# Kernel tuning notes

Hardware: AMD Instinct MI355X
Metric: run time of the kernel (lower is better)

## Reference

```python
import jax, jax.numpy as jnp
import numpy as np

J = 8      # number of octaves/scales
Q = 8      # first-order wavelets per octave (Q2 = 1 for second order)
T = 65536  # signal support
EPS = 1e-8
XI_MAX = 0.35  # highest wavelet center frequency (cycles/sample)


def _build_filters(N=T, J_=J, Q_=Q):
    """Morlet-like analytic filterbank defined directly in the Fourier domain."""
    f = np.fft.fftfreq(N)  # normalized freqs in [-0.5, 0.5)
    # first-order: J*Q log-spaced bandpass filters
    xis1 = XI_MAX * 2.0 ** (-np.arange(J_ * Q_) / Q_)
    sig1 = xis1 / Q_
    psi1 = np.exp(-0.5 * ((f[None, :] - xis1[:, None]) / sig1[:, None]) ** 2)
    j1 = np.arange(J_ * Q_) // Q_  # octave index of each first-order filter
    # second-order: one wavelet per octave (Q2=1)
    xis2 = XI_MAX * 2.0 ** (-np.arange(J_).astype(np.float64))
    sig2 = 0.6 * xis2
    psi2 = np.exp(-0.5 * ((f[None, :] - xis2[:, None]) / sig2[:, None]) ** 2)
    # low-pass at scale 2^J
    sig_phi = XI_MAX * 2.0 ** (-J_)
    phi = np.exp(-0.5 * (f / sig_phi) ** 2)
    return (jnp.asarray(psi1, jnp.float32), jnp.asarray(psi2, jnp.float32),
            jnp.asarray(phi, jnp.float32), j1)


def _scatter(x):
    """Order-0/1/2 wavelet scattering: FFT conv -> modulus -> low-pass -> subsample."""
    psi1, psi2, phi, j1 = _build_filters()
    stride = 2 ** J
    xf = jnp.fft.fft(x)  # [B, N] complex64
    lowpass = lambda uf: jnp.real(jnp.fft.ifft(uf * phi))[..., ::stride]
    S0 = lowpass(xf)[:, None, :]                                  # [B, 1, N/2^J]
    U1 = jnp.abs(jnp.fft.ifft(xf[:, None, :] * psi1[None]))      # [B, JQ, N]
    U1f = jnp.fft.fft(U1)
    S1 = lowpass(U1f)                                             # [B, JQ, N/2^J]
    parts = [S0, S1]
    for j2_ in range(J):  # small fixed loop over second-order scales
        sel = j1 < j2_    # static (numpy) frequency-ordering mask
        if not sel.any():
            continue
        U2 = jnp.abs(jnp.fft.ifft(U1f[:, sel] * psi2[j2_]))
        parts.append(lowpass(jnp.fft.fft(U2)))
    return jnp.concatenate(parts, axis=1)  # [B, 289, N/2^J]


def setup_inputs() -> dict:
    key = jax.random.key(0)
    x = jax.random.normal(key, (8, T), dtype=jnp.float32)
    return {"x": x}


def reference(x):
    Sx = _scatter(x)
    # kymatio Scattering1D has no `output_format` attr -> real=Sx, imag=0,
    # then log-magnitude normalization (normalize=True):
    mag = jnp.sqrt(Sx * Sx + EPS)
    real = jnp.log(mag + EPS)
    imag = jnp.zeros_like(real)
    return (real, imag)
```

## Files before the change

kernel.cpp:

```cpp
#include <hip/hip_runtime.h>
#include <hip/hip_fp16.h>
#include <math.h>

#define NN 65536
#define TWO_PI 6.283185307179586f
#define RSTR 264
#define SWZ(m) ((m) ^ (((m) >> 4) & 15))
#define SWZI(m, r) (SWZ(m) ^ ((r) & 12))
#define CTOT 10829824ul

__constant__ int CLO[8]  = {-32768, -15360, -5376, -8192, -8192, -2048, -2048, -2048};
__constant__ int CWW[8]  = {65536, 42240, 16384, 16384, 16384, 4096, 4096, 4096};
__constant__ int CRING[8] = {0, 0, 1, 1, 1, 1, 1, 1};
__constant__ unsigned long COFF[8] = {0ul, 4194304ul, 6897664ul, 7946240ul,
                                      8994816ul, 10043392ul, 10305536ul, 10567680ul};

__device__ __forceinline__ void lds_fence() {
    asm volatile("s_waitcnt lgkmcnt(0)" ::: "memory");
}
__device__ __forceinline__ int rev16(int p) { return ((p & 3) << 2) | (p >> 2); }
__device__ __forceinline__ int rev64(int p) { return ((p & 3) << 4) | (p & 12) | (p >> 4); }

__device__ __forceinline__ int quarter_mask(int klo, int khi)
{
    int qm = 0;
#pragma unroll
    for (int qq = 0; qq < 4; ++qq) {
        int lo_q = 16384 * qq - 255;
        int hi_q = 16384 * qq + 16639;
        bool act;
        if (klo >= 0) act = (hi_q >= klo) && (lo_q <= khi);
        else          act = (lo_q <= khi) || (hi_q >= klo + NN);
        if (act) qm |= (1 << qq);
    }
    return qm;
}

__device__ __forceinline__ void build_tw6(float* twt, int t)
{
    if (t < 16) {
        float s1, c1; __sincosf((TWO_PI / 64.0f) * (float)t, &s1, &c1);
        float c2 = c1 * c1 - s1 * s1, s2 = 2.f * c1 * s1;
        float c3 = c2 * c1 - s2 * s1, s3 = c2 * s1 + s2 * c1;
        float* e = twt + 6 * t;
        e[0] = c1; e[1] = s1; e[2] = c2; e[3] = s2; e[4] = c3; e[5] = s3;
    }
}

template<int SIGN>
__device__ __forceinline__ void fft16(float* xr, float* xi, float* yr, float* yi)
{
    const float S = (SIGN > 0) ? 1.0f : -1.0f;
    const float C8 = 0.92387953251f, S8 = 0.38268343236f, R2 = 0.70710678119f;
#pragma unroll
    for (int n0 = 0; n0 < 4; ++n0) {
        float z0r=xr[n0],    z0i=xi[n0];
        float z1r=xr[n0+4],  z1i=xi[n0+4];
        float z2r=xr[n0+8],  z2i=xi[n0+8];
        float z3r=xr[n0+12], z3i=xi[n0+12];
        float t0r=z0r+z2r, t0i=z0i+z2i;
        float t1r=z0r-z2r, t1i=z0i-z2i;
        float t2r=z1r+z3r, t2i=z1i+z3i;
        float t3r=S*(z1r-z3r), t3i=S*(z1i-z3i);
        xr[n0]=t0r+t2r;      xi[n0]=t0i+t2i;
        xr[n0+4]=t1r-t3i;    xi[n0+4]=t1i+t3r;
        xr[n0+8]=t0r-t2r;    xi[n0+8]=t0i-t2i;
        xr[n0+12]=t1r+t3i;   xi[n0+12]=t1i-t3r;
    }
    {
        const float W1r=C8,  W1i=S*S8;
        const float W2r=R2,  W2i=S*R2;
        const float W3r=S8,  W3i=S*C8;
        const float W6r=-R2, W6i=S*R2;
        const float W9r=-C8, W9i=-S*S8;
#define TWID(idx, wr, wi) { float ar=xr[idx], ai=xi[idx]; xr[idx]=ar*(wr)-ai*(wi); xi[idx]=ar*(wi)+ai*(wr); }
        TWID(5,W1r,W1i)  TWID(9,W2r,W2i)   TWID(13,W3r,W3i)
        TWID(6,W2r,W2i)  { float ar=xr[10], ai=xi[10]; xr[10]=-S*ai; xi[10]=S*ar; } TWID(14,W6r,W6i)
        TWID(7,W3r,W3i)  TWID(11,W6r,W6i)  TWID(15,W9r,W9i)
#undef TWID
    }
#pragma unroll
    for (int p = 0; p < 4; ++p) {
        float z0r=xr[4*p],   z0i=xi[4*p];
        float z1r=xr[4*p+1], z1i=xi[4*p+1];
        float z2r=xr[4*p+2], z2i=xi[4*p+2];
        float z3r=xr[4*p+3], z3i=xi[4*p+3];
        float t0r=z0r+z2r, t0i=z0i+z2i;
        float t1r=z0r-z2r, t1i=z0i-z2i;
        float t2r=z1r+z3r, t2i=z1i+z3i;
        float t3r=S*(z1r-z3r), t3i=S*(z1i-z3i);
        yr[p]=t0r+t2r;     yi[p]=t0i+t2i;
        yr[p+4]=t1r-t3i;   yi[p+4]=t1i+t3r;
        yr[p+8]=t0r-t2r;   yi[p+8]=t0i-t2i;
        yr[p+12]=t1r+t3i;  yi[p+12]=t1i-t3r;
    }
}

template<int SIGN, bool BIGTW, int OUT, bool INREAL, int PADL, int PADR>
__device__ __forceinline__ void fft256_soa(float* rr, float* ri, int u, int n1,
                                           float twrate, float mscale, int cxor, int qmask)
{
    float xr[16], xi[16], yr[16], yi[16];
#pragma unroll
    for (int qq = 0; qq < 4; ++qq) {
        if (qmask & (1 << qq)) {
#pragma unroll
            for (int j = 0; j < 4; ++j) {
                int b = qq * 4 + j;
                int s = SWZ(u + (b << 4)) ^ cxor;
                xr[b] = rr[s];
                xi[b] = INREAL ? 0.f : ri[s];
            }
        } else {
#pragma unroll
            for (int j = 0; j < 4; ++j) { xr[qq * 4 + j] = 0.f; xi[qq * 4 + j] = 0.f; }
        }
    }
    fft16<SIGN>(xr, xi, yr, yi);
    float sa, ca;
    __sincosf((float)SIGN * (TWO_PI / 256.0f) * (float)u, &sa, &ca);
    float twr = 1.f, twi = 0.f;
#pragma unroll
    for (int c = 0; c < 16; ++c) {
        int s = SWZ((c << 4) + u) ^ cxor;
        rr[s] = yr[c] * twr - yi[c] * twi;
        ri[s] = yr[c] * twi + yi[c] * twr;
        float nr = twr * ca - twi * sa; twi = twr * sa + twi * ca; twr = nr;
    }
    lds_fence();
#pragma unroll
    for (int a = 0; a < 16; ++a) {
        int s = SWZ((u << 4) + a) ^ cxor;
        xr[a] = rr[s]; xi[a] = ri[s];
    }
    fft16<SIGN>(xr, xi, yr, yi);
    float tbr = 1.f, tbi = 0.f, str = 1.f, sti = 0.f;
    if (BIGTW) {
        float s0, c0, s1, c1;
        __sincosf((float)SIGN * twrate * (float)(n1 * u), &s0, &c0);
        __sincosf((float)SIGN * twrate * (float)(n1 << 4), &s1, &c1);
        tbr = c0; tbi = s0; str = c1; sti = s1;
    }
#pragma unroll
    for (int d = 0; d < 16; ++d) {
        float vr = yr[d], vi = yi[d];
        if (BIGTW) {
            float pr = vr * tbr - vi * tbi, pi = vr * tbi + vi * tbr;
            vr = pr; vi = pi;
            float nr = tbr * str - tbi * sti; tbi = tbr * sti + tbi * str; tbr = nr;
        }
        int k = u + (d << 4);
        if (OUT == 1) {
            rr[SWZ(k) ^ cxor] = sqrtf(fmaf(vr, vr, vi * vi)) * mscale;
        } else if (OUT == 2) {
            float mag = sqrtf(fmaf(vr, vr, vi * vi)) * mscale;
            ri[PADL + k] = mag;
            if (k >= 256 - PADL) ri[k - (256 - PADL)] = mag;
            if (k < PADR) ri[PADL + 256 + k] = mag;
        } else {
            int s = SWZ(k) ^ cxor;
            rr[s] = vr; ri[s] = vi;
        }
    }
    lds_fence();
}

template<int L, int CLOG, int RST, int SIGN, bool SWZC>
__device__ __forceinline__ void lds_dit(float* re, float* im, const float* twt, int t, int T)
{
    const float S = (float)SIGN;
    const int NC = 1 << CLOG;
    const int nbf = NC * (L >> 2);
    for (int h = 1; h < L; h <<= 2) {
        __syncthreads();
        for (int i = t; i < nbf; i += T) {
            int c = i & (NC - 1);
            int bf = i >> CLOG;
            int j = bf & (h - 1);
            int q0 = ((bf - j) << 2) + j;
            int r0 = q0, r1 = q0 + h, r2 = q0 + 2 * h, r3 = q0 + 3 * h;
            int a0, a1, a2, a3;
            if (SWZC) {
                a0 = r0 * RST + SWZI(c, r0); a1 = r1 * RST + SWZI(c, r1);
                a2 = r2 * RST + SWZI(c, r2); a3 = r3 * RST + SWZI(c, r3);
            } else {
                a0 = r0 * RST + c; a1 = r1 * RST + c; a2 = r2 * RST + c; a3 = r3 * RST + c;
            }
            float x0r = re[a0], x0i = im[a0];
            float x1r = re[a1], x1i = im[a1];
            float x2r = re[a2], x2i = im[a2];
            float x3r = re[a3], x3i = im[a3];
            if (h > 1) {
                const float* e = twt + 6 * (j * (16 / h));
                float cj = e[0], sj = S * e[1];
                float c2 = e[2], s2 = S * e[3];
                float c3 = e[4], s3 = S * e[5];
                float r;
                r = x1r * cj - x1i * sj; x1i = x1r * sj + x1i * cj; x1r = r;
                r = x2r * c2 - x2i * s2; x2i = x2r * s2 + x2i * c2; x2r = r;
                r = x3r * c3 - x3i * s3; x3i = x3r * s3 + x3i * c3; x3r = r;
            }
            float t0r = x0r + x2r, t0i = x0i + x2i;
            float t1r = x0r - x2r, t1i = x0i - x2i;
            float t2r = x1r + x3r, t2i = x1i + x3i;
            float t3r = -S * (x1i - x3i), t3i = S * (x1r - x3r);
            re[a0] = t0r + t2r; im[a0] = t0i + t2i;
            re[a1] = t1r + t3r; im[a1] = t1i + t3i;
            re[a2] = t0r - t2r; im[a2] = t0i - t2i;
            re[a3] = t1r - t3r; im[a3] = t1i - t3i;
        }
    }
    __syncthreads();
}

template<int L, int CLOG, int RST, int SIGN, bool SWZC>
__device__ __forceinline__ void lds_dif(float* re, float* im, const float* twt, int t, int T)
{
    const float S = (float)SIGN;
    const int NC = 1 << CLOG;
    const int nbf = NC * (L >> 2);
    for (int h = L >> 2; h >= 1; h >>= 2) {
        __syncthreads();
        for (int i = t; i < nbf; i += T) {
            int c = i & (NC - 1);
            int bf = i >> CLOG;
            int j = bf & (h - 1);
            int q0 = ((bf - j) << 2) + j;
            int r0 = q0, r1 = q0 + h, r2 = q0 + 2 * h, r3 = q0 + 3 * h;
            int a0, a1, a2, a3;
            if (SWZC) {
                a0 = r0 * RST + SWZI(c, r0); a1 = r1 * RST + SWZI(c, r1);
                a2 = r2 * RST + SWZI(c, r2); a3 = r3 * RST + SWZI(c, r3);
            } else {
                a0 = r0 * RST + c; a1 = r1 * RST + c; a2 = r2 * RST + c; a3 = r3 * RST + c;
            }
            float x0r = re[a0], x0i = im[a0];
            float x1r = re[a1], x1i = im[a1];
            float x2r = re[a2], x2i = im[a2];
            float x3r = re[a3], x3i = im[a3];
            float t0r = x0r + x2r, t0i = x0i + x2i;
            float t1r = x0r - x2r, t1i = x0i - x2i;
            float t2r = x1r + x3r, t2i = x1i + x3i;
            float t3r = -S * (x1i - x3i), t3i = S * (x1r - x3r);
            float y1r = t1r + t3r, y1i = t1i + t3i;
            float y2r = t0r - t2r, y2i = t0i - t2i;
            float y3r = t1r - t3r, y3i = t1i - t3i;
            re[a0] = t0r + t2r; im[a0] = t0i + t2i;
            if (h > 1) {
                const float* e = twt + 6 * (j * (16 / h));
                float cj = e[0], sj = S * e[1];
                float c2 = e[2], s2 = S * e[3];
                float c3 = e[4], s3 = S * e[5];
                re[a1] = y1r * cj - y1i * sj; im[a1] = y1r * sj + y1i * cj;
                re[a2] = y2r * c2 - y2i * s2; im[a2] = y2r * s2 + y2i * c2;
                re[a3] = y3r * c3 - y3i * s3; im[a3] = y3r * s3 + y3i * c3;
            } else {
                re[a1] = y1r; im[a1] = y1i;
                re[a2] = y2r; im[a2] = y2i;
                re[a3] = y3r; im[a3] = y3i;
            }
        }
    }
    __syncthreads();
}

__global__ __launch_bounds__(256)
void xf_stage1(const float* __restrict__ x, float2* __restrict__ D)
{
    __shared__ float sre[16 * RSTR];
    __shared__ float sim[16 * RSTR];
    const int t = threadIdx.x;
    const int r = blockIdx.x >> 4;
    const int n10 = (blockIdx.x & 15) << 4;
#pragma unroll
    for (int it = 0; it < 16; ++it) {
        int flat = it * 256 + t;
        int i = flat & 15, n2 = flat >> 4;
        int n = (n10 + i) + (n2 << 8);
        sre[i * RSTR + SWZI(n2, i)] = x[(size_t)r * NN + n];
        sim[i * RSTR + SWZI(n2, i)] = 0.f;
    }
    __syncthreads();
    const int g = t >> 4, u = t & 15;
    fft256_soa<-1, true, 0, false, 0, 0>(sre + g * RSTR, sim + g * RSTR, u, n10 + g,
                                         TWO_PI / (float)NN, 1.f, g & 12, 15);
    __syncthreads();
#pragma unroll
    for (int it = 0; it < 16; ++it) {
        int flat = it * 256 + t;
        int i = flat & 15, k2 = flat >> 4;
        int s = i * RSTR + SWZI(k2, i);
        D[(size_t)r * NN + (k2 << 8) + (n10 + i)] = make_float2(sre[s], sim[s]);
    }
}

__global__ __launch_bounds__(256)
void xf_stage2(const float2* __restrict__ D, float2* __restrict__ XF)
{
    __shared__ float sre[16 * RSTR];
    __shared__ float sim[16 * RSTR];
    const int t = threadIdx.x;
    const int r = blockIdx.x >> 4;
    const int k20 = (blockIdx.x & 15) << 4;
#pragma unroll
    for (int it = 0; it < 16; ++it) {
        float2 v = D[(size_t)r * NN + ((size_t)(k20 + it) << 8) + t];
        sre[it * RSTR + SWZI(t, it)] = v.x;
        sim[it * RSTR + SWZI(t, it)] = v.y;
    }
    __syncthreads();
    const int g = t >> 4, u = t & 15;
    fft256_soa<-1, false, 0, false, 0, 0>(sre + g * RSTR, sim + g * RSTR, u, 0, 0.f, 1.f, g & 12, 15);
    __syncthreads();
#pragma unroll
    for (int it = 0; it < 16; ++it) {
        int flat = it * 256 + t;
        int fi = flat & 15, k1 = flat >> 4;
        int s = fi * RSTR + SWZI(k1, fi);
        XF[(size_t)r * NN + (size_t)(k20 + fi) + ((size_t)k1 << 8)] = make_float2(sre[s], sim[s]);
    }
}

__device__ void d_fo_stage1(float* sm, int t, int blk, const float2* __restrict__ XF,
                            __half2* __restrict__ Dh)
{
    float* sre = sm; float* sim = sm + 4224;
    const int r = blk >> 4;
    const int n10 = (blk & 15) << 4;
    const int q = r;
    const int j1 = q >> 6, ql = q & 63;
    const int srow = ql >> 3, w = ql & 7;
    const int lam = j1 * 8 + w;
    const float xi = 0.35f * exp2f(-(float)lam * 0.125f);
    const float invsig = 8.0f / xi;
    const float kc = xi * (float)NN;
    const float Hh = 5.0f * (xi * 0.125f) * (float)NN;
    const int klo = (int)(kc - Hh), khi = (int)(kc + Hh) + 1;
    const int qm = (khi >= NN) ? 15 : quarter_mask(klo, khi);
#pragma unroll
    for (int it = 0; it < 16; ++it) {
        int i = t & 15, n2 = (it << 4) + (t >> 4);
        if (!(qm & (1 << (it >> 2)))) {
            sre[i * RSTR + SWZI(n2, i)] = 0.f;
            sim[i * RSTR + SWZI(n2, i)] = 0.f;
            continue;
        }
        int n = (n10 + i) + (n2 << 8);
        float nsf = (float)((n < NN / 2) ? n : n - NN);
        float vr = 0.f, vi = 0.f;
        if (fabsf(nsf - kc) <= Hh) {
            float2 v = XF[(size_t)srow * NN + n];
            float a = (nsf * (1.0f / (float)NN) - xi) * invsig;
            float wg = __expf(-0.5f * a * a) * 0.0625f;
            vr = v.x * wg; vi = v.y * wg;
        }
        sre[i * RSTR + SWZI(n2, i)] = vr;
        sim[i * RSTR + SWZI(n2, i)] = vi;
    }
    __syncthreads();
    const int g = t >> 4, u = t & 15;
    fft256_soa<1, true, 0, false, 0, 0>(sre + g * RSTR, sim + g * RSTR, u, n10 + g,
                                        TWO_PI / (float)NN, 1.f, g & 12, qm);
    __syncthreads();
#pragma unroll
    for (int it = 0; it < 16; ++it) {
        int flat = it * 256 + t;
        int i = flat & 15, k2 = flat >> 4;
        int s = i * RSTR + SWZI(k2, i);
        Dh[(size_t)r * NN + (k2 << 8) + (n10 + i)] = __floats2half2_rn(sre[s], sim[s]);
    }
}

__device__ void d_fo_mid(float* sm, int t, int blk, const __half2* __restrict__ Dh,
                         __half2* __restrict__ D2h)
{
    float* sre = sm; float* sim = sm + 4224;
    const int r = blk >> 4;
    const int k20 = (blk & 15) << 4;
#pragma unroll
    for (int it = 0; it < 16; ++it) {
        float2 v = __half22float2(Dh[(size_t)r * NN + ((size_t)(k20 + it) << 8) + t]);
        sre[it * RSTR + SWZI(t, it)] = v.x;
        sim[it * RSTR + SWZI(t, it)] = v.y;
    }
    __syncthreads();
    const int g = t >> 4, u = t & 15;
    float* rr = sre + g * RSTR; float* ri = sim + g * RSTR;
    fft256_soa<1, false, 1, false, 0, 0>(rr, ri, u, 0, 0.f, 16.0f / (float)NN, g & 12, 15);
    fft256_soa<-1, true, 0, true, 0, 0>(rr, ri, u, k20 + g, TWO_PI / (float)NN, 1.f, g & 12, 15);
    __syncthreads();
#pragma unroll
    for (int it = 0; it < 16; ++it) {
        int flat = it * 256 + t;
        int i = flat & 15, k2 = flat >> 4;
        int s = i * RSTR + SWZI(k2, i);
        D2h[(size_t)r * NN + (k2 << 8) + (k20 + i)] = __floats2half2_rn(sre[s], sim[s]);
    }
}

__device__ void d_fo_stage2(float* sm, int t, int blk, const __half2* __restrict__ D2h,
                            __half2* __restrict__ Cw)
{
    float* sre = sm; float* sim = sm + 4224;
    const int r = blk >> 4;
    const int k20 = (blk & 15) << 4;
    const int j1 = r >> 6, ql = r & 63;
#pragma unroll
    for (int it = 0; it < 16; ++it) {
        float2 v = __half22float2(D2h[(size_t)r * NN + ((size_t)(k20 + it) << 8) + t]);
        sre[it * RSTR + SWZI(t, it)] = v.x;
        sim[it * RSTR + SWZI(t, it)] = v.y;
    }
    __syncthreads();
    const int g = t >> 4, u = t & 15;
    fft256_soa<-1, false, 0, false, 0, 0>(sre + g * RSTR, sim + g * RSTR, u, 0, 0.f, 1.f, g & 12, 15);
    __syncthreads();
    const size_t base = COFF[j1] + (size_t)ql * CWW[j1];
    const int lo = CLO[j1], Wd = CWW[j1];
#pragma unroll
    for (int it = 0; it < 16; ++it) {
        int flat = it * 256 + t;
        int fi = flat & 15, k1 = flat >> 4;
        int k = (k20 + fi) + (k1 << 8);
        int ksg = (k < NN / 2) ? k : k - NN;
        int idx = ksg - lo;
        if (idx >= 0 && idx < Wd) {
            int s = fi * RSTR + SWZI(k1, fi);
            Cw[base + idx] = __floats2half2_rn(sre[s], sim[s]);
        }
    }
}

__device__ void d_sfold(float* sm, int t, int blk, const float2* __restrict__ XF,
                        const __half2* __restrict__ Cw, float* __restrict__ out)
{
    float* Gr = sm; float* Gi = sm + 256;
    const float invsigphi = 731.428571f;
    float ar = 0.f, ai = 0.f;
    if (blk < 8) {
#pragma unroll
        for (int qq = -4; qq <= 4; ++qq) {
            int ks = t + (qq << 8);
            int k = ks & (NN - 1);
            float a = ((float)ks * (1.0f / (float)NN)) * invsigphi;
            float wg = __expf(-0.5f * a * a);
            float2 v = XF[(size_t)blk * NN + k];
            ar = fmaf(v.x, wg, ar); ai = fmaf(v.y, wg, ai);
        }
    } else {
        int q = blk - 8;
        int j1 = q >> 6, ql = q & 63;
        size_t base = COFF[j1] + (size_t)ql * CWW[j1];
        int lo = CLO[j1], Wd = CWW[j1], ring = CRING[j1];
#pragma unroll
        for (int qq = -4; qq <= 4; ++qq) {
            int ks = t + (qq << 8);
            float a = ((float)ks * (1.0f / (float)NN)) * invsigphi;
            float wg = __expf(-0.5f * a * a);
            int idx = ring ? ((ks - lo) & (Wd - 1)) : (ks - lo);
            float2 v = __half22float2(Cw[base + idx]);
            ar = fmaf(v.x, wg, ar); ai = fmaf(v.y, wg, ai);
        }
    }
    Gr[t] = ar; Gi[t] = ai;
    __syncthreads();
    float sb, cb;
    __sincosf((TWO_PI / 256.0f) * (float)t, &sb, &cb);
    float wr = 1.f, wi = 0.f, s = 0.f;
    for (int kk = 0; kk < 256; ++kk) {
        s = fmaf(Gr[kk], wr, s);
        s = fmaf(-Gi[kk], wi, s);
        float nr = wr * cb - wi * sb; wi = wr * sb + wi * cb; wr = nr;
    }
    s *= (1.0f / (float)NN);
    float mag = sqrtf(fmaf(s, s, 1e-8f));
    float val = logf(mag + 1e-8f);
    int b, chan;
    if (blk < 8) { b = blk; chan = 0; }
    else { int q = blk - 8; int j1 = q >> 6, ql = q & 63; b = ql >> 3; chan = 1 + j1 * 8 + (ql & 7); }
    out[((size_t)b * 289 + chan) * 256 + t] = val;
}

__device__ __forceinline__ void so_decode_full(int q, int& j1, int& j2, int& rb)
{
    int pp = q >> 6;
    rb = q & 63;
    j2 = (pp == 0) ? 1 : 2;
    j1 = (pp == 0) ? 0 : pp - 1;
}
__device__ __forceinline__ void so_decode_dec16(int q, int& j1, int& j2, int& rb)
{
    int pp = q >> 6;
    rb = q & 63;
    j2 = (pp < 3) ? 3 : 4;
    j1 = (pp < 3) ? pp : pp - 3;
}

__device__ void d_so_stage1(float* sm, int t, int blk, const __half2* __restrict__ Cw,
                            __half2* __restrict__ Dh)
{
    float* sre = sm; float* sim = sm + 4224;
    const int r = blk >> 4;
    const int n10 = (blk & 15) << 4;
    int j1, j2, rb;
    so_decode_full(r, j1, j2, rb);
    const float xi2 = 0.35f * exp2f(-(float)j2);
    const float invsig = 1.0f / (0.6f * xi2);
    const float kc = xi2 * (float)NN;
    const float Hh = 5.0f * (0.6f * xi2) * (float)NN;
    const int klo = (int)(kc - Hh), khi = (int)(kc + Hh) + 1;
    const int qm = (klo >= 0 && khi >= NN) ? 15 : quarter_mask(klo, khi);
    const size_t base = COFF[j1] + (size_t)rb * CWW[j1];
    const int lo = CLO[j1], Wd = CWW[j1];
#pragma unroll
    for (int it = 0; it < 16; ++it) {
        int i = t & 15, n2 = (it << 4) + (t >> 4);
        if (!(qm & (1 << (it >> 2)))) {
            sre[i * RSTR + SWZI(n2, i)] = 0.f;
            sim[i * RSTR + SWZI(n2, i)] = 0.f;
            continue;
        }
        int n = (n10 + i) + (n2 << 8);
        int ksg = (n < NN / 2) ? n : n - NN;
        float nsf = (float)ksg;
        float vr = 0.f, vi = 0.f;
        int idx = ksg - lo;
        if (fabsf(nsf - kc) <= Hh && idx >= 0 && idx < Wd) {
            float2 v = __half22float2(Cw[base + idx]);
            float a = (nsf * (1.0f / (float)NN) - xi2) * invsig;
            float wg = __expf(-0.5f * a * a) * (1.0f / 256.0f);
            vr = v.x * wg; vi = v.y * wg;
        }
        sre[i * RSTR + SWZI(n2, i)] = vr;
        sim[i * RSTR + SWZI(n2, i)] = vi;
    }
    __syncthreads();
    const int g = t >> 4, u = t & 15;
    fft256_soa<1, true, 0, false, 0, 0>(sre + g * RSTR, sim + g * RSTR, u, n10 + g,
                                        TWO_PI / (float)NN, 1.f, g & 12, qm);
    __syncthreads();
#pragma unroll
    for (int it = 0; it < 16; ++it) {
        int flat = it * 256 + t;
        int i = flat & 15, k2 = flat >> 4;
        int s = i * RSTR + SWZI(k2, i);
        Dh[(size_t)r * NN + (k2 << 8) + (n10 + i)] = __floats2half2_rn(sre[s], sim[s]);
    }
}

__device__ void d_so_stage2(float* sm, int t, int blk, const __half2* __restrict__ Dh,
                            float* __restrict__ S2acc)
{
    float* sre = sm; float* sim = sm + 4224;
    float* wtab = sm + 8448;
    const int r = blk >> 4;
    const int k20 = (blk & 15) << 4;
#pragma unroll
    for (int it = 0; it < 16; ++it) {
        float2 v = __half22float2(Dh[(size_t)r * NN + ((size_t)(k20 + it) << 8) + t]);
        sre[it * RSTR + SWZI(t, it)] = v.x;
        sim[it * RSTR + SWZI(t, it)] = v.y;
    }
    if (t < 128) {
        int fi = t >> 3, dd = (t & 7) - 4;
        int w = k20 + fi + (dd << 8) + 768;
        float val = 0.f;
        if (w >= 0 && w <= 1536) {
            float m = (float)(w - 768);
            val = 0.003426963f * __expf(-3.690276e-5f * m * m);
        }
        wtab[fi * 8 + (t & 7)] = val;
    }
    __syncthreads();
    const int g = t >> 4, u = t & 15;
    fft256_soa<1, false, 2, false, 4, 3>(sre + g * RSTR, sim + g * RSTR, u, 0, 0.f, 1.f, g & 12, 15);
    __syncthreads();
    float acc = 0.f;
#pragma unroll
    for (int fi = 0; fi < 16; ++fi) {
        const float* row = sim + fi * RSTR;
#pragma unroll
        for (int dd = 0; dd < 8; ++dd)
            acc = fmaf(row[t + dd], wtab[fi * 8 + dd], acc);
    }
    atomicAdd(&S2acc[(size_t)r * 256 + t], acc * (1.0f / 256.0f));
}

template<int MODE>
__device__ void d_dec16_s1(float* sm, int t, int blk, const float2* __restrict__ XF,
                           const __half2* __restrict__ Cw, __half2* __restrict__ Dh16)
{
    float* sre = sm; float* sim = sm + 4096; float* twt = sm + 8192;
    const int r = blk >> 2;
    const int c0 = (blk & 3) << 6;
    const int q = r;
    float xi, invsig, kc, Hh; int srow = 0; size_t cbase = 0; int lo = 0, Wd = 0, ring = 0;
    if (MODE == 1) {
        int j1 = 2 + (q >> 6); int ql = q & 63; srow = ql >> 3;
        int lam = j1 * 8 + (ql & 7);
        xi = 0.35f * exp2f(-(float)lam * 0.125f);
        invsig = 8.0f / xi; kc = xi * (float)NN; Hh = 6.10f * (xi * 0.125f) * (float)NN;
    } else {
        int j1, j2, rb;
        so_decode_dec16(q, j1, j2, rb);
        xi = 0.35f * exp2f(-(float)j2);
        invsig = 1.0f / (0.6f * xi); kc = xi * (float)NN;
        Hh = fminf(6.10f * (0.6f * xi) * (float)NN, 7967.0f);
        cbase = COFF[j1] + (size_t)rb * CWW[j1]; lo = CLO[j1]; Wd = CWW[j1]; ring = CRING[j1];
    }
    build_tw6(twt, t);
    const int klo = (int)ceilf(kc - Hh);
#pragma unroll
    for (int it = 0; it < 16; ++it) {
        int flat = it * 256 + t;
        int c = flat & 63, n2 = flat >> 6;
        int kap = (c0 + c) + (n2 << 8);
        int kk = klo + (int)(((unsigned)(kap - klo)) & 16383u);
        float vr = 0.f, vi = 0.f;
        if (fabsf((float)kk - kc) <= Hh) {
            float2 v;
            bool ok = true;
            if (MODE == 1) v = XF[(size_t)srow * NN + (kk & (NN - 1))];
            else {
                int idx;
                if (ring) idx = (kk - lo) & (Wd - 1);
                else { idx = kk - lo; ok = (idx >= 0 && idx < Wd); }
                v = ok ? __half22float2(Cw[cbase + idx]) : make_float2(0.f, 0.f);
            }
            float a = ((float)kk * (1.0f / (float)NN) - xi) * invsig;
            float wg = __expf(-0.5f * a * a) * 0.015625f;
            vr = v.x * wg; vi = v.y * wg;
        }
        int p = rev64(n2);
        sre[(p << 6) + c] = vr;
        sim[(p << 6) + c] = vi;
    }
    lds_dit<64, 6, 64, 1, false>(sre, sim, twt, t, 256);
    {
        const int c = t & 63, r0 = t >> 6;
        float sA, cA, sD, cD;
        __sincosf((TWO_PI / 16384.0f) * (float)(r0 * (c0 + c)), &sA, &cA);
        __sincosf((TWO_PI / 16384.0f) * (float)(4 * (c0 + c)), &sD, &cD);
#pragma unroll
        for (int it = 0; it < 16; ++it) {
            int row = (it << 2) + r0;
            int a = (row << 6) + c;
            float rr = sre[a] * cA - sim[a] * sA;
            sim[a] = sre[a] * sA + sim[a] * cA; sre[a] = rr;
            float nc = cA * cD - sA * sD; sA = cA * sD + sA * cD; cA = nc;
        }
    }
    __syncthreads();
#pragma unroll
    for (int it = 0; it < 16; ++it) {
        int flat = it * 256 + t;
        int c = flat & 63, row = flat >> 6;
        Dh16[(size_t)r * 16384 + (row << 8) + (c0 + c)] =
            __floats2half2_rn(sre[(row << 6) + c], sim[(row << 6) + c]);
    }
}

__device__ void d_dec16_s2so(float* sm, int t, int blk, const __half2* __restrict__ Dh16,
                             float* __restrict__ S2acc)
{
    float* sre = sm; float* sim = sm + 4224;
    float* wtab = sm + 8448;
    const int r = blk >> 2;
    const int k2base = (blk & 3) << 4;
#pragma unroll
    for (int it = 0; it < 16; ++it) {
        float2 v = __half22float2(Dh16[(size_t)r * 16384 + ((k2base + it) << 8) + t]);
        sre[it * RSTR + SWZI(t, it)] = v.x;
        sim[it * RSTR + SWZI(t, it)] = v.y;
    }
    if (t < 96) {
        int p = t / 6, dl = t % 6;
        float w = (float)(256 * (dl - 2) - 4 * (k2base + p));
        wtab[p * 6 + dl] = 0.003426963f * __expf(-3.690276e-5f * w * w);
    }
    __syncthreads();
    const int g = t >> 4, u = t & 15;
    fft256_soa<1, false, 2, false, 3, 2>(sre + g * RSTR, sim + g * RSTR, u, 0, 0.f,
                                         64.0f / (float)NN, g & 12, 15);
    __syncthreads();
    float acc = 0.f;
#pragma unroll
    for (int p = 0; p < 16; ++p) {
        const float* row = sim + p * RSTR;
#pragma unroll
        for (int dl = 0; dl < 6; ++dl)
            acc = fmaf(row[t + 5 - dl], wtab[p * 6 + dl], acc);
    }
    atomicAdd(&S2acc[(size_t)(192 + r) * 256 + t], acc * 4.0f);
}

__device__ void d_dec16_s2fo(float* sm, int t, int blk, const __half2* __restrict__ Dh16,
                             __half2* __restrict__ D2h16)
{
    float* sre = sm; float* sim = sm + 4224;
    const int r = blk >> 2;
    const int k2base = (blk & 3) << 4;
#pragma unroll
    for (int it = 0; it < 16; ++it) {
        float2 v = __half22float2(Dh16[(size_t)r * 16384 + ((k2base + it) << 8) + t]);
        sre[it * RSTR + SWZI(t, it)] = v.x;
        sim[it * RSTR + SWZI(t, it)] = v.y;
    }
    __syncthreads();
    const int g = t >> 4, u = t & 15;
    float* rr = sre + g * RSTR; float* ri = sim + g * RSTR;
    fft256_soa<1, false, 1, false, 0, 0>(rr, ri, u, 0, 0.f, 256.0f / (float)NN, g & 12, 15);
    fft256_soa<-1, true, 0, true, 0, 0>(rr, ri, u, k2base + g, TWO_PI / 16384.0f, 1.f, g & 12, 15);
    __syncthreads();
#pragma unroll
    for (int it = 0; it < 16; ++it) {
        int a = it * RSTR + SWZI(t, it);
        D2h16[(size_t)r * 16384 + ((k2base + it) << 8) + t] = __floats2half2_rn(sre[a], sim[a]);
    }
}

__device__ void d_dec16_s3fo(float* sm, int t, int blk, const __half2* __restrict__ D2h16,
                             __half2* __restrict__ Cw)
{
    float* sre = sm; float* sim = sm + 4096; float* twt = sm + 8192;
    const int r = blk >> 2;
    const int c0 = (blk & 3) << 6;
    const int j1 = 2 + (r >> 6), ql = r & 63;
    build_tw6(twt, t);
#pragma unroll
    for (int it = 0; it < 16; ++it) {
        int flat = it * 256 + t;
        int c = flat & 63, m2 = flat >> 6;
        float2 v = __half22float2(D2h16[(size_t)r * 16384 + (m2 << 8) + (c0 + c)]);
        sre[(m2 << 6) + c] = v.x;
        sim[(m2 << 6) + c] = v.y;
    }
    lds_dif<64, 6, 64, -1, false>(sre, sim, twt, t, 256);
    const int lo = CLO[j1];
    const size_t rbase = COFF[j1] + (size_t)ql * 16384;
#pragma unroll
    for (int it = 0; it < 16; ++it) {
        int flat = it * 256 + t;
        int c = flat & 63, p = flat >> 6;
        int kap = (c0 + c) + (rev64(p) << 8);
        int ks = (kap < 8192) ? kap : kap - 16384;
        int idx = (ks - lo) & 16383;
        int a = (p << 6) + c;
        Cw[rbase + idx] = __floats2half2_rn(sre[a], sim[a]);
    }
}

__device__ void d_m4k_fo(float* sm, int t, int blk, const float2* __restrict__ XF,
                         __half2* __restrict__ Cw)
{
    float* sre = sm; float* sim = sm + 4224; float* twt = sm + 8448;
    const int q = blk;
    const int j1 = 5 + (q >> 6), ql = q & 63;
    const int srow = ql >> 3;
    const int lam = j1 * 8 + (ql & 7);
    const float xi = 0.35f * exp2f(-(float)lam * 0.125f);
    const float invsig = 8.0f / xi;
    const float kc = xi * (float)NN;
    const float Hh = 6.10f * (xi * 0.125f) * (float)NN;
    const int klo = (int)ceilf(kc - Hh);
    build_tw6(twt, t);
#pragma unroll
    for (int it = 0; it < 16; ++it) {
        int kap = t + (it << 8);
        int kk = klo + (int)(((unsigned)(kap - klo)) & 4095u);
        float vr = 0.f, vi = 0.f;
        if (fabsf((float)kk - kc) <= Hh) {
            float2 v = XF[(size_t)srow * NN + (kk & (NN - 1))];
            float a = ((float)kk * (1.0f / (float)NN) - xi) * invsig;
            float wg = __expf(-0.5f * a * a);
            vr = v.x * wg; vi = v.y * wg;
        }
        int p = rev16(it);
        sre[p * RSTR + SWZI(t, p)] = vr;
        sim[p * RSTR + SWZI(t, p)] = vi;
    }
    lds_dit<16, 8, RSTR, 1, true>(sre, sim, twt, t, 256);
    {
        float sD, cD; __sincosf((TWO_PI / 4096.0f) * (float)t, &sD, &cD);
        float cA = 1.f, sA = 0.f;
#pragma unroll
        for (int it = 0; it < 16; ++it) {
            int a = it * RSTR + SWZI(t, it);
            float rr = sre[a] * cA - sim[a] * sA;
            sim[a] = sre[a] * sA + sim[a] * cA; sre[a] = rr;
            float nc = cA * cD - sA * sD; sA = cA * sD + sA * cD; cA = nc;
        }
    }
    __syncthreads();
    const int g = t >> 4, u = t & 15;
    float* rr = sre + g * RSTR; float* ri = sim + g * RSTR;
    fft256_soa<1, false, 1, false, 0, 0>(rr, ri, u, 0, 0.f, 16.0f / (float)NN, g & 12, 15);
    fft256_soa<-1, true, 0, true, 0, 0>(rr, ri, u, g, TWO_PI / 4096.0f, 1.f, g & 12, 15);
    lds_dif<16, 8, RSTR, -1, true>(sre, sim, twt, t, 256);
    const int lo = CLO[j1];
    const size_t rbase = COFF[j1] + (size_t)ql * 4096;
#pragma unroll
    for (int it = 0; it < 16; ++it) {
        int kap = t + (rev16(it) << 8);
        int ks = (kap < 2048) ? kap : kap - 4096;
        int idx = (ks - lo) & 4095;
        int a = it * RSTR + SWZI(t, it);
        Cw[rbase + idx] = __floats2half2_rn(sre[a], sim[a]);
    }
}

__device__ void d_m4k_so(float* sm, int t, int blk, const __half2* __restrict__ Cw,
                         float* __restrict__ out)
{
    float* sre = sm; float* sim = sm + 4224;
    float* twt = sm + 8448; float* wtab = sm + 8544;
    const int q = blk;
    const int pp = q >> 6, rb = q & 63;
    int j1, j2;
    if (pp < 5)       { j2 = 5; j1 = pp; }
    else if (pp < 11) { j2 = 6; j1 = pp - 5; }
    else              { j2 = 7; j1 = pp - 11; }
    const float xi2 = 0.35f * exp2f(-(float)j2);
    const float invsig = 1.0f / (0.6f * xi2);
    const float kc = xi2 * (float)NN;
    const float Hh = fminf(6.10f * (0.6f * xi2) * (float)NN, 1823.0f);
    const int klo = (int)ceilf(kc - Hh);
    const size_t cbase = COFF[j1] + (size_t)rb * CWW[j1];
    const int lo = CLO[j1], Wd = CWW[j1], ring = CRING[j1];
    build_tw6(twt, t);
#pragma unroll
    for (int it = 0; it < 16; ++it) {
        int kap = t + (it << 8);
        int kk = klo + (int)(((unsigned)(kap - klo)) & 4095u);
        float vr = 0.f, vi = 0.f;
        if (fabsf((float)kk - kc) <= Hh) {
            int idx; bool ok = true;
            if (ring) idx = (kk - lo) & (Wd - 1);
            else { idx = kk - lo; ok = (idx >= 0 && idx < Wd); }
            if (ok) {
                float2 v = __half22float2(Cw[cbase + idx]);
                float a = ((float)kk * (1.0f / (float)NN) - xi2) * invsig;
                float wg = __expf(-0.5f * a * a);
                vr = v.x * wg; vi = v.y * wg;
            }
        }
        int p = rev16(it);
        sre[p * RSTR + SWZI(t, p)] = vr;
        sim[p * RSTR + SWZI(t, p)] = vi;
    }
    if (t < 96) {
        int p = t / 6, dl = t % 6;
        float w = (float)(256 * (dl - 2) - 16 * p);
        wtab[p * 6 + dl] = 0.003426963f * __expf(-3.690276e-5f * w * w);
    }
    lds_dit<16, 8, RSTR, 1, true>(sre, sim, twt, t, 256);
    {
        float sD, cD; __sincosf((TWO_PI / 4096.0f) * (float)t, &sD, &cD);
        float cA = 1.f, sA = 0.f;
#pragma unroll
        for (int it = 0; it < 16; ++it) {
            int a = it * RSTR + SWZI(t, it);
            float rr = sre[a] * cA - sim[a] * sA;
            sim[a] = sre[a] * sA + sim[a] * cA; sre[a] = rr;
            float nc = cA * cD - sA * sD; sA = cA * sD + sA * cD; cA = nc;
        }
    }
    __syncthreads();
    const int g = t >> 4, u = t & 15;
    fft256_soa<1, false, 2, false, 3, 2>(sre + g * RSTR, sim + g * RSTR, u, 0, 0.f,
                                         1.0f / (float)NN, g & 12, 15);
    __syncthreads();
    float acc = 0.f;
#pragma unroll
    for (int p = 0; p < 16; ++p) {
        const float* row = sim + p * RSTR;
#pragma unroll
        for (int dl = 0; dl < 6; ++dl)
            acc = fmaf(row[t + 5 - dl], wtab[p * 6 + dl], acc);
    }
    acc *= 16.0f;
    const int b = rb >> 3;
    const int chan = 65 + 4 * j2 * (j2 - 1) + j1 * 8 + (rb & 7);
    float mag = sqrtf(fmaf(acc, acc, 1e-8f));
    out[((size_t)b * 289 + chan) * 256 + t] = logf(mag + 1e-8f);
}

__global__ __launch_bounds__(256)
void fo_s1_kernel(const float2* __restrict__ XF, __half2* __restrict__ Cw,
                  __half2* __restrict__ DhB, __half2* __restrict__ Dh16)
{
    __shared__ float sm[8704];
    const int t = threadIdx.x;
    const int b = blockIdx.x;
    if (b < 192) d_m4k_fo(sm, t, b, XF, Cw);
    else if (b < 960) d_dec16_s1<1>(sm, t, b - 192, XF, nullptr, Dh16);
    else d_fo_stage1(sm, t, b - 960, XF, DhB);
}

__global__ __launch_bounds__(256)
void fo_s2_kernel(const __half2* __restrict__ DhB, const __half2* __restrict__ Dh16,
                  __half2* __restrict__ D2h, __half2* __restrict__ D2h16)
{
    __shared__ float sm[8704];
    const int t = threadIdx.x;
    const int b = blockIdx.x;
    if (b < 768) d_dec16_s2fo(sm, t, b, Dh16, D2h16);
    else d_fo_mid(sm, t, b - 768, DhB, D2h);
}

__global__ __launch_bounds__(256)
void fo_s3_kernel(const __half2* __restrict__ D2h, const __half2* __restrict__ D2h16,
                  __half2* __restrict__ Cw)
{
    __shared__ float sm[8704];
    const int t = threadIdx.x;
    const int b = blockIdx.x;
    if (b < 768) d_dec16_s3fo(sm, t, b, D2h16, Cw);
    else d_fo_stage2(sm, t, b - 768, D2h, Cw);
}

__global__ __launch_bounds__(256)
void so_1_kernel(const float2* __restrict__ XF, const __half2* __restrict__ Cw,
                 __half2* __restrict__ DhS, __half2* __restrict__ Dh16so,
                 float* __restrict__ out)
{
    __shared__ float sm[8704];
    const int t = threadIdx.x;
    const int b = blockIdx.x;
    if (b < 1152) d_m4k_so(sm, t, b, Cw, out);
    else if (b < 2944) d_dec16_s1<2>(sm, t, b - 1152, nullptr, Cw, Dh16so);
    else if (b < 6016) d_so_stage1(sm, t, b - 2944, Cw, DhS);
    else d_sfold(sm, t, b - 6016, XF, Cw, out);
}

__global__ __launch_bounds__(256)
void so_2_kernel(const __half2* __restrict__ DhS, const __half2* __restrict__ Dh16so,
                 float* __restrict__ S2acc)
{
    __shared__ float sm[8704];
    const int t = threadIdx.x;
    const int b = blockIdx.x;
    if (b < 1792) d_dec16_s2so(sm, t, b, Dh16so, S2acc);
    else d_so_stage2(sm, t, b - 1792, DhS, S2acc);
}

__global__ __launch_bounds__(256)
void s2final(const float* __restrict__ S2acc, float* __restrict__ out)
{
    const int q = blockIdx.x, n = threadIdx.x;
    int j1, j2, rb;
    if (q < 192) so_decode_full(q, j1, j2, rb);
    else         so_decode_dec16(q - 192, j1, j2, rb);
    const int b = rb >> 3;
    const int chan = 65 + 4 * j2 * (j2 - 1) + j1 * 8 + (rb & 7);
    float s = S2acc[(size_t)q * 256 + n];
    float mag = sqrtf(fmaf(s, s, 1e-8f));
    out[((size_t)b * 289 + chan) * 256 + n] = logf(mag + 1e-8f);
}

__global__ void zero2_kernel(float* a, int na, float* b, int nb)
{
    int i = blockIdx.x * 256 + threadIdx.x;
    if (i < na) a[i] = 0.f;
    else if (i < na + nb) b[i - na] = 0.f;
}

extern "C" void kernel_launch(void* const* d_in, const int* in_sizes, int n_in,
                              void* d_out, int out_size, void* d_ws, size_t ws_size,
                              hipStream_t stream)
{
    const float* x = (const float*)d_in[0];
    float* out = (float*)d_out;
    char* ws = (char*)d_ws;

    size_t off = 0;
    float2*  XF    = (float2*)ws;                 off += 8ul * NN * 8;
    __half2* Cw    = (__half2*)(ws + off);        off += CTOT * 4ul;
    float*   S2acc = (float*)(ws + off);          off += 640ul * 256 * 4;
    off = (off + 255) & ~255ul;
    char* sc = ws + off;

    __half2* DhB   = (__half2*)sc;
    __half2* D2h   = (__half2*)(sc + 33554432ul);
    __half2* Dh16  = (__half2*)(sc + 67108864ul);
    __half2* D2h16 = (__half2*)(sc + 79691776ul);
    __half2* DhS    = (__half2*)sc;
    __half2* Dh16so = (__half2*)(sc + 50331648ul);
    float2*  Df     = (float2*)sc;

    {
        int nz = 8 * 289 * 256;
        int na = 640 * 256;
        zero2_kernel<<<(nz + na + 255) / 256, 256, 0, stream>>>(out + nz, nz, S2acc, na);
    }

    xf_stage1<<<8 * 16, 256, 0, stream>>>(x, Df);
    xf_stage2<<<8 * 16, 256, 0, stream>>>(Df, XF);

    fo_s1_kernel<<<3008, 256, 0, stream>>>(XF, Cw, DhB, Dh16);
    fo_s2_kernel<<<2816, 256, 0, stream>>>(DhB, Dh16, D2h, D2h16);
    fo_s3_kernel<<<2816, 256, 0, stream>>>(D2h, D2h16, Cw);

    so_1_kernel<<<6536, 256, 0, stream>>>(XF, Cw, DhS, Dh16so, out);
    so_2_kernel<<<4864, 256, 0, stream>>>(DhS, Dh16so, S2acc);
    s2final<<<640, 256, 0, stream>>>(S2acc, out);
}
```

Before: 257.6 us.

## Store FFT scratch in LDS as packed half2 and fold zeroing into first FFT

The intermediate FFT stages now keep their data in shared memory as packed __half2 values instead of split float real/imag arrays. This halves the LDS footprint, which goes from 8704 to 4480 floats per block, so more blocks can be resident per CU. It also lets global half2 data move to and from LDS with no conversion. Separately, the zeroing kernel is merged into the first input FFT kernel as extra blocks, which removes one launch. The cost is extra fp16 rounding at every intra-LDS butterfly pass, which lowers accuracy, plus convert instructions inside the FFT loops.

```diff
diff --git a/kernel.cpp b/kernel.cpp
--- a/kernel.cpp
+++ b/kernel.cpp
@@ -4,7 +4,7 @@
 
 #define NN 65536
 #define TWO_PI 6.283185307179586f
-#define RSTR 264
+#define HRSTR 264
 #define SWZ(m) ((m) ^ (((m) >> 4) & 15))
 #define SWZI(m, r) (SWZ(m) ^ ((r) & 12))
 #define CTOT 10829824ul
@@ -20,6 +20,10 @@
 }
 __device__ __forceinline__ int rev16(int p) { return ((p & 3) << 2) | (p >> 2); }
 __device__ __forceinline__ int rev64(int p) { return ((p & 3) << 4) | (p & 12) | (p >> 4); }
+__device__ __forceinline__ float2 h2f(__half2 h) { return __half22float2(h); }
+__device__ __forceinline__ __half2 f2h(float a, float b) {
+    return __floats2half2_rn(a, b);
+}
 
 __device__ __forceinline__ int quarter_mask(int klo, int khi)
 {
@@ -96,9 +100,9 @@
     }
 }
 
-template<int SIGN, bool BIGTW, int OUT, bool INREAL, int PADL, int PADR>
-__device__ __forceinline__ void fft256_soa(float* rr, float* ri, int u, int n1,
-                                           float twrate, float mscale, int cxor, int qmask)
+template<int SIGN, bool BIGTW, int OUT, int PADL, int PADR>
+__device__ __forceinline__ void fft256_pk(__half2* row, int u, int n1,
+                                          float twrate, float mscale, int cxor, int qmask)
 {
     float xr[16], xi[16], yr[16], yi[16];
 #pragma unroll
@@ -107,9 +111,8 @@
 #pragma unroll
             for (int j = 0; j < 4; ++j) {
                 int b = qq * 4 + j;
-                int s = SWZ(u + (b << 4)) ^ cxor;
-                xr[b] = rr[s];
-                xi[b] = INREAL ? 0.f : ri[s];
+                float2 v = h2f(row[SWZ(u + (b << 4)) ^ cxor]);
+                xr[b] = v.x; xi[b] = v.y;
             }
         } else {
 #pragma unroll
@@ -122,16 +125,15 @@
     float twr = 1.f, twi = 0.f;
 #pragma unroll
     for (int c = 0; c < 16; ++c) {
-        int s = SWZ((c << 4) + u) ^ cxor;
-        rr[s] = yr[c] * twr - yi[c] * twi;
-        ri[s] = yr[c] * twi + yi[c] * twr;
+        row[SWZ((c << 4) + u) ^ cxor] = f2h(yr[c] * twr - yi[c] * twi,
+                                            yr[c] * twi + yi[c] * twr);
         float nr = twr * ca - twi * sa; twi = twr * sa + twi * ca; twr = nr;
     }
     lds_fence();
 #pragma unroll
     for (int a = 0; a < 16; ++a) {
-        int s = SWZ((u << 4) + a) ^ cxor;
-        xr[a] = rr[s]; xi[a] = ri[s];
+        float2 v = h2f(row[SWZ((u << 4) + a) ^ cxor]);
+        xr[a] = v.x; xi[a] = v.y;
     }
     fft16<SIGN>(xr, xi, yr, yi);
     float tbr = 1.f, tbi = 0.f, str = 1.f, sti = 0.f;
@@ -151,22 +153,22 @@
         }
         int k = u + (d << 4);
         if (OUT == 1) {
-            rr[SWZ(k) ^ cxor] = sqrtf(fmaf(vr, vr, vi * vi)) * mscale;
+            row[SWZ(k) ^ cxor] = f2h(sqrtf(fmaf(vr, vr, vi * vi)) * mscale, 0.f);
         } else if (OUT == 2) {
             float mag = sqrtf(fmaf(vr, vr, vi * vi)) * mscale;
-            ri[PADL + k] = mag;
-            if (k >= 256 - PADL) ri[k - (256 - PADL)] = mag;
-            if (k < PADR) ri[PADL + 256 + k] = mag;
+            float* rf = (float*)row;
+            rf[PADL + k] = mag;
+            if (k >= 256 - PADL) rf[k - (256 - PADL)] = mag;
+            if (k < PADR) rf[PADL + 256 + k] = mag;
         } else {
-            int s = SWZ(k) ^ cxor;
-            rr[s] = vr; ri[s] = vi;
+            row[SWZ(k) ^ cxor] = f2h(vr, vi);
         }
     }
     lds_fence();
 }
 
 template<int L, int CLOG, int RST, int SIGN, bool SWZC>
-__device__ __forceinline__ void lds_dit(float* re, float* im, const float* twt, int t, int T)
+__device__ __forceinline__ void lds_dit_pk(__half2* pl, const float* twt, int t, int T)
 {
     const float S = (float)SIGN;
     const int NC = 1 << CLOG;
@@ -186,10 +188,10 @@
             } else {
                 a0 = r0 * RST + c; a1 = r1 * RST + c; a2 = r2 * RST + c; a3 = r3 * RST + c;
             }
-            float x0r = re[a0], x0i = im[a0];
-            float x1r = re[a1], x1i = im[a1];
-            float x2r = re[a2], x2i = im[a2];
-            float x3r = re[a3], x3i = im[a3];
+            float2 z0 = h2f(pl[a0]), z1 = h2f(pl[a1]);
+            float2 z2 = h2f(pl[a2]), z3 = h2f(pl[a3]);
+            float x0r=z0.x, x0i=z0.y, x1r=z1.x, x1i=z1.y;
+            float x2r=z2.x, x2i=z2.y, x3r=z3.x, x3i=z3.y;
             if (h > 1) {
                 const float* e = twt + 6 * (j * (16 / h));
                 float cj = e[0], sj = S * e[1];
@@ -204,17 +206,17 @@
             float t1r = x0r - x2r, t1i = x0i - x2i;
             float t2r = x1r + x3r, t2i = x1i + x3i;
             float t3r = -S * (x1i - x3i), t3i = S * (x1r - x3r);
-            re[a0] = t0r + t2r; im[a0] = t0i + t2i;
-            re[a1] = t1r + t3r; im[a1] = t1i + t3i;
-            re[a2] = t0r - t2r; im[a2] = t0i - t2i;
-            re[a3] = t1r - t3r; im[a3] = t1i - t3i;
+            pl[a0] = f2h(t0r + t2r, t0i + t2i);
+            pl[a1] = f2h(t1r + t3r, t1i + t3i);
+            pl[a2] = f2h(t0r - t2r, t0i - t2i);
+            pl[a3] = f2h(t1r - t3r, t1i - t3i);
         }
     }
     __syncthreads();
 }
 
 template<int L, int CLOG, int RST, int SIGN, bool SWZC>
-__device__ __forceinline__ void lds_dif(float* re, float* im, const float* twt, int t, int T)
+__device__ __forceinline__ void lds_dif_pk(__half2* pl, const float* twt, int t, int T)
 {
     const float S = (float)SIGN;
     const int NC = 1 << CLOG;
@@ -234,10 +236,10 @@
             } else {
                 a0 = r0 * RST + c; a1 = r1 * RST + c; a2 = r2 * RST + c; a3 = r3 * RST + c;
             }
-            float x0r = re[a0], x0i = im[a0];
-            float x1r = re[a1], x1i = im[a1];
-            float x2r = re[a2], x2i = im[a2];
-            float x3r = re[a3], x3i = im[a3];
+            float2 z0 = h2f(pl[a0]), z1 = h2f(pl[a1]);
+            float2 z2 = h2f(pl[a2]), z3 = h2f(pl[a3]);
+            float x0r=z0.x, x0i=z0.y, x1r=z1.x, x1i=z1.y;
+            float x2r=z2.x, x2i=z2.y, x3r=z3.x, x3i=z3.y;
             float t0r = x0r + x2r, t0i = x0i + x2i;
             float t1r = x0r - x2r, t1i = x0i - x2i;
             float t2r = x1r + x3r, t2i = x1i + x3i;
@@ -245,51 +247,108 @@
             float y1r = t1r + t3r, y1i = t1i + t3i;
             float y2r = t0r - t2r, y2i = t0i - t2i;
             float y3r = t1r - t3r, y3i = t1i - t3i;
-            re[a0] = t0r + t2r; im[a0] = t0i + t2i;
+            pl[a0] = f2h(t0r + t2r, t0i + t2i);
             if (h > 1) {
                 const float* e = twt + 6 * (j * (16 / h));
                 float cj = e[0], sj = S * e[1];
                 float c2 = e[2], s2 = S * e[3];
                 float c3 = e[4], s3 = S * e[5];
-                re[a1] = y1r * cj - y1i * sj; im[a1] = y1r * sj + y1i * cj;
-                re[a2] = y2r * c2 - y2i * s2; im[a2] = y2r * s2 + y2i * c2;
-                re[a3] = y3r * c3 - y3i * s3; im[a3] = y3r * s3 + y3i * c3;
+                pl[a1] = f2h(y1r * cj - y1i * sj, y1r * sj + y1i * cj);
+                pl[a2] = f2h(y2r * c2 - y2i * s2, y2r * s2 + y2i * c2);
+                pl[a3] = f2h(y3r * c3 - y3i * s3, y3r * s3 + y3i * c3);
             } else {
-                re[a1] = y1r; im[a1] = y1i;
-                re[a2] = y2r; im[a2] = y2i;
-                re[a3] = y3r; im[a3] = y3i;
+                pl[a1] = f2h(y1r, y1i);
+                pl[a2] = f2h(y2r, y2i);
+                pl[a3] = f2h(y3r, y3i);
             }
         }
     }
     __syncthreads();
 }
 
+template<int SIGN, bool BIGTW>
+__device__ __forceinline__ void fft256_f32(float* rr, float* ri, int u, int n1,
+                                           float twrate, int cxor)
+{
+    float xr[16], xi[16], yr[16], yi[16];
+#pragma unroll
+    for (int b = 0; b < 16; ++b) {
+        int s = SWZ(u + (b << 4)) ^ cxor;
+        xr[b] = rr[s]; xi[b] = ri[s];
+    }
+    fft16<SIGN>(xr, xi, yr, yi);
+    float sa, ca;
+    __sincosf((float)SIGN * (TWO_PI / 256.0f) * (float)u, &sa, &ca);
+    float twr = 1.f, twi = 0.f;
+#pragma unroll
+    for (int c = 0; c < 16; ++c) {
+        int s = SWZ((c << 4) + u) ^ cxor;
+        rr[s] = yr[c] * twr - yi[c] * twi;
+        ri[s] = yr[c] * twi + yi[c] * twr;
+        float nr = twr * ca - twi * sa; twi = twr * sa + twi * ca; twr = nr;
+    }
+    lds_fence();
+#pragma unroll
+    for (int a = 0; a < 16; ++a) {
+        int s = SWZ((u << 4) + a) ^ cxor;
+        xr[a] = rr[s]; xi[a] = ri[s];
+    }
+    fft16<SIGN>(xr, xi, yr, yi);
+    float tbr = 1.f, tbi = 0.f, str = 1.f, sti = 0.f;
+    if (BIGTW) {
+        float s0, c0, s1, c1;
+        __sincosf((float)SIGN * twrate * (float)(n1 * u), &s0, &c0);
+        __sincosf((float)SIGN * twrate * (float)(n1 << 4), &s1, &c1);
+        tbr = c0; tbi = s0; str = c1; sti = s1;
+    }
+#pragma unroll
+    for (int d = 0; d < 16; ++d) {
+        float vr = yr[d], vi = yi[d];
+        if (BIGTW) {
+            float pr = vr * tbr - vi * tbi, pi = vr * tbi + vi * tbr;
+            vr = pr; vi = pi;
+            float nr = tbr * str - tbi * sti; tbi = tbr * sti + tbi * str; tbr = nr;
+        }
+        int s = SWZ(u + (d << 4)) ^ cxor;
+        rr[s] = vr; ri[s] = vi;
+    }
+    lds_fence();
+}
+
 __global__ __launch_bounds__(256)
-void xf_stage1(const float* __restrict__ x, float2* __restrict__ D)
-{
-    __shared__ float sre[16 * RSTR];
-    __shared__ float sim[16 * RSTR];
+void xfz_kernel(const float* __restrict__ x, float2* __restrict__ D,
+                float* __restrict__ outImag, int nz, float* __restrict__ S2acc, int na)
+{
+    __shared__ float sre[16 * HRSTR];
+    __shared__ float sim[16 * HRSTR];
     const int t = threadIdx.x;
-    const int r = blockIdx.x >> 4;
-    const int n10 = (blockIdx.x & 15) << 4;
+    const int blk = blockIdx.x;
+    if (blk >= 128) {
+        int i = (blk - 128) * 256 + t;
+        if (i < nz) outImag[i] = 0.f;
+        else if (i < nz + na) S2acc[i - nz] = 0.f;
+        return;
+    }
+    const int r = blk >> 4;
+    const int n10 = (blk & 15) << 4;
 #pragma unroll
     for (int it = 0; it < 16; ++it) {
         int flat = it * 256 + t;
         int i = flat & 15, n2 = flat >> 4;
         int n = (n10 + i) + (n2 << 8);
-        sre[i * RSTR + SWZI(n2, i)] = x[(size_t)r * NN + n];
-        sim[i * RSTR + SWZI(n2, i)] = 0.f;
+        sre[i * HRSTR + SWZI(n2, i)] = x[(size_t)r * NN + n];
+        sim[i * HRSTR + SWZI(n2, i)] = 0.f;
     }
     __syncthreads();
     const int g = t >> 4, u = t & 15;
-    fft256_soa<-1, true, 0, false, 0, 0>(sre + g * RSTR, sim + g * RSTR, u, n10 + g,
-                                         TWO_PI / (float)NN, 1.f, g & 12, 15);
+    fft256_f32<-1, true>(sre + g * HRSTR, sim + g * HRSTR, u, n10 + g,
+                         TWO_PI / (float)NN, g & 12);
     __syncthreads();
 #pragma unroll
     for (int it = 0; it < 16; ++it) {
         int flat = it * 256 + t;
         int i = flat & 15, k2 = flat >> 4;
-        int s = i * RSTR + SWZI(k2, i);
+        int s = i * HRSTR + SWZI(k2, i);
         D[(size_t)r * NN + (k2 << 8) + (n10 + i)] = make_float2(sre[s], sim[s]);
     }
 }
@@ -297,38 +356,39 @@
 __global__ __launch_bounds__(256)
 void xf_stage2(const float2* __restrict__ D, float2* __restrict__ XF)
 {
-    __shared__ float sre[16 * RSTR];
-    __shared__ float sim[16 * RSTR];
+    __shared__ float sre[16 * HRSTR];
+    __shared__ float sim[16 * HRSTR];
     const int t = threadIdx.x;
     const int r = blockIdx.x >> 4;
     const int k20 = (blockIdx.x & 15) << 4;
 #pragma unroll
     for (int it = 0; it < 16; ++it) {
         float2 v = D[(size_t)r * NN + ((size_t)(k20 + it) << 8) + t];
-        sre[it * RSTR + SWZI(t, it)] = v.x;
-        sim[it * RSTR + SWZI(t, it)] = v.y;
+        sre[it * HRSTR + SWZI(t, it)] = v.x;
+        sim[it * HRSTR + SWZI(t, it)] = v.y;
     }
     __syncthreads();
     const int g = t >> 4, u = t & 15;
-    fft256_soa<-1, false, 0, false, 0, 0>(sre + g * RSTR, sim + g * RSTR, u, 0, 0.f, 1.f, g & 12, 15);
+    fft256_f32<-1, false>(sre + g * HRSTR, sim + g * HRSTR, u, 0, 0.f, g & 12);
     __syncthreads();
 #pragma unroll
     for (int it = 0; it < 16; ++it) {
         int flat = it * 256 + t;
         int fi = flat & 15, k1 = flat >> 4;
-        int s = fi * RSTR + SWZI(k1, fi);
+        int s = fi * HRSTR + SWZI(k1, fi);
         XF[(size_t)r * NN + (size_t)(k20 + fi) + ((size_t)k1 << 8)] = make_float2(sre[s], sim[s]);
     }
 }
 
-__device__ void d_fo_stage1(float* sm, int t, int blk, const float2* __restrict__ XF,
+#define SM_FLOATS 4480
+
+__device__ void d_fo_stage1(float* smf, int t, int blk, const float2* __restrict__ XF,
                             __half2* __restrict__ Dh)
 {
-    float* sre = sm; float* sim = sm + 4224;
+    __half2* sld = (__half2*)smf;
     const int r = blk >> 4;
     const int n10 = (blk & 15) << 4;
-    const int q = r;
-    const int j1 = q >> 6, ql = q & 63;
+    const int j1 = r >> 6, ql = r & 63;
     const int srow = ql >> 3, w = ql & 7;
     const int lam = j1 * 8 + w;
     const float xi = 0.35f * exp2f(-(float)lam * 0.125f);
@@ -341,8 +401,7 @@
     for (int it = 0; it < 16; ++it) {
         int i = t & 15, n2 = (it << 4) + (t >> 4);
         if (!(qm & (1 << (it >> 2)))) {
-            sre[i * RSTR + SWZI(n2, i)] = 0.f;
-            sim[i * RSTR + SWZI(n2, i)] = 0.f;
+            sld[i * HRSTR + SWZI(n2, i)] = f2h(0.f, 0.f);
             continue;
         }
         int n = (n10 + i) + (n2 << 8);
@@ -354,66 +413,57 @@
             float wg = __expf(-0.5f * a * a) * 0.0625f;
             vr = v.x * wg; vi = v.y * wg;
         }
-        sre[i * RSTR + SWZI(n2, i)] = vr;
-        sim[i * RSTR + SWZI(n2, i)] = vi;
+        sld[i * HRSTR + SWZI(n2, i)] = f2h(vr, vi);
     }
     __syncthreads();
     const int g = t >> 4, u = t & 15;
-    fft256_soa<1, true, 0, false, 0, 0>(sre + g * RSTR, sim + g * RSTR, u, n10 + g,
-                                        TWO_PI / (float)NN, 1.f, g & 12, qm);
+    fft256_pk<1, true, 0, 0, 0>(sld + g * HRSTR, u, n10 + g, TWO_PI / (float)NN, 1.f,
+                                g & 12, qm);
     __syncthreads();
 #pragma unroll
     for (int it = 0; it < 16; ++it) {
         int flat = it * 256 + t;
         int i = flat & 15, k2 = flat >> 4;
-        int s = i * RSTR + SWZI(k2, i);
-        Dh[(size_t)r * NN + (k2 << 8) + (n10 + i)] = __floats2half2_rn(sre[s], sim[s]);
-    }
-}
-
-__device__ void d_fo_mid(float* sm, int t, int blk, const __half2* __restrict__ Dh,
+        Dh[(size_t)r * NN + (k2 << 8) + (n10 + i)] = sld[i * HRSTR + SWZI(k2, i)];
+    }
+}
+
+__device__ void d_fo_mid(float* smf, int t, int blk, const __half2* __restrict__ Dh,
                          __half2* __restrict__ D2h)
 {
-    float* sre = sm; float* sim = sm + 4224;
+    __half2* sld = (__half2*)smf;
     const int r = blk >> 4;
     const int k20 = (blk & 15) << 4;
 #pragma unroll
-    for (int it = 0; it < 16; ++it) {
-        float2 v = __half22float2(Dh[(size_t)r * NN + ((size_t)(k20 + it) << 8) + t]);
-        sre[it * RSTR + SWZI(t, it)] = v.x;
-        sim[it * RSTR + SWZI(t, it)] = v.y;
-    }
+    for (int it = 0; it < 16; ++it)
+        sld[it * HRSTR + SWZI(t, it)] = Dh[(size_t)r * NN + ((size_t)(k20 + it) << 8) + t];
     __syncthreads();
     const int g = t >> 4, u = t & 15;
-    float* rr = sre + g * RSTR; float* ri = sim + g * RSTR;
-    fft256_soa<1, false, 1, false, 0, 0>(rr, ri, u, 0, 0.f, 16.0f / (float)NN, g & 12, 15);
-    fft256_soa<-1, true, 0, true, 0, 0>(rr, ri, u, k20 + g, TWO_PI / (float)NN, 1.f, g & 12, 15);
+    __half2* row = sld + g * HRSTR;
+    fft256_pk<1, false, 1, 0, 0>(row, u, 0, 0.f, 16.0f / (float)NN, g & 12, 15);
+    fft256_pk<-1, true, 0, 0, 0>(row, u, k20 + g, TWO_PI / (float)NN, 1.f, g & 12, 15);
     __syncthreads();
 #pragma unroll
     for (int it = 0; it < 16; ++it) {
         int flat = it * 256 + t;
         int i = flat & 15, k2 = flat >> 4;
-        int s = i * RSTR + SWZI(k2, i);
-        D2h[(size_t)r * NN + (k2 << 8) + (k20 + i)] = __floats2half2_rn(sre[s], sim[s]);
-    }
-}
-
-__device__ void d_fo_stage2(float* sm, int t, int blk, const __half2* __restrict__ D2h,
+        D2h[(size_t)r * NN + (k2 << 8) + (k20 + i)] = sld[i * HRSTR + SWZI(k2, i)];
+    }
+}
+
+__device__ void d_fo_stage2(float* smf, int t, int blk, const __half2* __restrict__ D2h,
                             __half2* __restrict__ Cw)
 {
-    float* sre = sm; float* sim = sm + 4224;
+    __half2* sld = (__half2*)smf;
     const int r = blk >> 4;
     const int k20 = (blk & 15) << 4;
     const int j1 = r >> 6, ql = r & 63;
 #pragma unroll
-    for (int it = 0; it < 16; ++it) {
-        float2 v = __half22float2(D2h[(size_t)r * NN + ((size_t)(k20 + it) << 8) + t]);
-        sre[it * RSTR + SWZI(t, it)] = v.x;
-        sim[it * RSTR + SWZI(t, it)] = v.y;
-    }
+    for (int it = 0; it < 16; ++it)
+        sld[it * HRSTR + SWZI(t, it)] = D2h[(size_t)r * NN + ((size_t)(k20 + it) << 8) + t];
     __syncthreads();
     const int g = t >> 4, u = t & 15;
-    fft256_soa<-1, false, 0, false, 0, 0>(sre + g * RSTR, sim + g * RSTR, u, 0, 0.f, 1.f, g & 12, 15);
+    fft256_pk<-1, false, 0, 0, 0>(sld + g * HRSTR, u, 0, 0.f, 1.f, g & 12, 15);
     __syncthreads();
     const size_t base = COFF[j1] + (size_t)ql * CWW[j1];
     const int lo = CLO[j1], Wd = CWW[j1];
@@ -424,17 +474,15 @@
         int k = (k20 + fi) + (k1 << 8);
         int ksg = (k < NN / 2) ? k : k - NN;
         int idx = ksg - lo;
-        if (idx >= 0 && idx < Wd) {
-            int s = fi * RSTR + SWZI(k1, fi);
-            Cw[base + idx] = __floats2half2_rn(sre[s], sim[s]);
-        }
-    }
-}
-
-__device__ void d_sfold(float* sm, int t, int blk, const float2* __restrict__ XF,
+        if (idx >= 0 && idx < Wd)
+            Cw[base + idx] = sld[fi * HRSTR + SWZI(k1, fi)];
+    }
+}
+
+__device__ void d_sfold(float* smf, int t, int blk, const float2* __restrict__ XF,
                         const __half2* __restrict__ Cw, float* __restrict__ out)
 {
-    float* Gr = sm; float* Gi = sm + 256;
+    float* Gr = smf; float* Gi = smf + 256;
     const float invsigphi = 731.428571f;
     float ar = 0.f, ai = 0.f;
     if (blk < 8) {
@@ -458,7 +506,7 @@
             float a = ((float)ks * (1.0f / (float)NN)) * invsigphi;
             float wg = __expf(-0.5f * a * a);
             int idx = ring ? ((ks - lo) & (Wd - 1)) : (ks - lo);
-            float2 v = __half22float2(Cw[base + idx]);
+            float2 v = h2f(Cw[base + idx]);
             ar = fmaf(v.x, wg, ar); ai = fmaf(v.y, wg, ai);
         }
     }
@@ -496,10 +544,10 @@
     j1 = (pp < 3) ? pp : pp - 3;
 }
 
-__device__ void d_so_stage1(float* sm, int t, int blk, const __half2* __restrict__ Cw,
+__device__ void d_so_stage1(float* smf, int t, int blk, const __half2* __restrict__ Cw,
                             __half2* __restrict__ Dh)
 {
-    float* sre = sm; float* sim = sm + 4224;
+    __half2* sld = (__half2*)smf;
     const int r = blk >> 4;
     const int n10 = (blk & 15) << 4;
     int j1, j2, rb;
@@ -516,8 +564,7 @@
     for (int it = 0; it < 16; ++it) {
         int i = t & 15, n2 = (it << 4) + (t >> 4);
         if (!(qm & (1 << (it >> 2)))) {
-            sre[i * RSTR + SWZI(n2, i)] = 0.f;
-            sim[i * RSTR + SWZI(n2, i)] = 0.f;
+            sld[i * HRSTR + SWZI(n2, i)] = f2h(0.f, 0.f);
             continue;
         }
         int n = (n10 + i) + (n2 << 8);
@@ -526,41 +573,36 @@
         float vr = 0.f, vi = 0.f;
         int idx = ksg - lo;
         if (fabsf(nsf - kc) <= Hh && idx >= 0 && idx < Wd) {
-            float2 v = __half22float2(Cw[base + idx]);
+            float2 v = h2f(Cw[base + idx]);
             float a = (nsf * (1.0f / (float)NN) - xi2) * invsig;
             float wg = __expf(-0.5f * a * a) * (1.0f / 256.0f);
             vr = v.x * wg; vi = v.y * wg;
         }
-        sre[i * RSTR + SWZI(n2, i)] = vr;
-        sim[i * RSTR + SWZI(n2, i)] = vi;
+        sld[i * HRSTR + SWZI(n2, i)] = f2h(vr, vi);
     }
     __syncthreads();
     const int g = t >> 4, u = t & 15;
-    fft256_soa<1, true, 0, false, 0, 0>(sre + g * RSTR, sim + g * RSTR, u, n10 + g,
-                                        TWO_PI / (float)NN, 1.f, g & 12, qm);
+    fft256_pk<1, true, 0, 0, 0>(sld + g * HRSTR, u, n10 + g, TWO_PI / (float)NN, 1.f,
+                                g & 12, qm);
     __syncthreads();
 #pragma unroll
     for (int it = 0; it < 16; ++it) {
         int flat = it * 256 + t;
         int i = flat & 15, k2 = flat >> 4;
-        int s = i * RSTR + SWZI(k2, i);
-        Dh[(size_t)r * NN + (k2 << 8) + (n10 + i)] = __floats2half2_rn(sre[s], sim[s]);
-    }
-}
-
-__device__ void d_so_stage2(float* sm, int t, int blk, const __half2* __restrict__ Dh,
+        Dh[(size_t)r * NN + (k2 << 8) + (n10 + i)] = sld[i * HRSTR + SWZI(k2, i)];
+    }
+}
+
+__device__ void d_so_stage2(float* smf, int t, int blk, const __half2* __restrict__ Dh,
                             float* __restrict__ S2acc)
 {
-    float* sre = sm; float* sim = sm + 4224;
-    float* wtab = sm + 8448;
+    __half2* sld = (__half2*)smf;
+    float* wtab = smf + 4320;
     const int r = blk >> 4;
     const int k20 = (blk & 15) << 4;
 #pragma unroll
-    for (int it = 0; it < 16; ++it) {
-        float2 v = __half22float2(Dh[(size_t)r * NN + ((size_t)(k20 + it) << 8) + t]);
-        sre[it * RSTR + SWZI(t, it)] = v.x;
-        sim[it * RSTR + SWZI(t, it)] = v.y;
-    }
+    for (int it = 0; it < 16; ++it)
+        sld[it * HRSTR + SWZI(t, it)] = Dh[(size_t)r * NN + ((size_t)(k20 + it) << 8) + t];
     if (t < 128) {
         int fi = t >> 3, dd = (t & 7) - 4;
         int w = k20 + fi + (dd << 8) + 768;
@@ -573,12 +615,12 @@
     }
     __syncthreads();
     const int g = t >> 4, u = t & 15;
-    fft256_soa<1, false, 2, false, 4, 3>(sre + g * RSTR, sim + g * RSTR, u, 0, 0.f, 1.f, g & 12, 15);
+    fft256_pk<1, false, 2, 4, 3>(sld + g * HRSTR, u, 0, 0.f, 1.f, g & 12, 15);
     __syncthreads();
     float acc = 0.f;
 #pragma unroll
     for (int fi = 0; fi < 16; ++fi) {
-        const float* row = sim + fi * RSTR;
+        const float* row = (const float*)(sld + fi * HRSTR);
 #pragma unroll
         for (int dd = 0; dd < 8; ++dd)
             acc = fmaf(row[t + dd], wtab[fi * 8 + dd], acc);
@@ -587,22 +629,22 @@
 }
 
 template<int MODE>
-__device__ void d_dec16_s1(float* sm, int t, int blk, const float2* __restrict__ XF,
+__device__ void d_dec16_s1(float* smf, int t, int blk, const float2* __restrict__ XF,
                            const __half2* __restrict__ Cw, __half2* __restrict__ Dh16)
 {
-    float* sre = sm; float* sim = sm + 4096; float* twt = sm + 8192;
+    __half2* sld = (__half2*)smf;
+    float* twt = smf + 4224;
     const int r = blk >> 2;
     const int c0 = (blk & 3) << 6;
-    const int q = r;
     float xi, invsig, kc, Hh; int srow = 0; size_t cbase = 0; int lo = 0, Wd = 0, ring = 0;
     if (MODE == 1) {
-        int j1 = 2 + (q >> 6); int ql = q & 63; srow = ql >> 3;
+        int j1 = 2 + (r >> 6); int ql = r & 63; srow = ql >> 3;
         int lam = j1 * 8 + (ql & 7);
         xi = 0.35f * exp2f(-(float)lam * 0.125f);
         invsig = 8.0f / xi; kc = xi * (float)NN; Hh = 6.10f * (xi * 0.125f) * (float)NN;
     } else {
         int j1, j2, rb;
-        so_decode_dec16(q, j1, j2, rb);
+        so_decode_dec16(r, j1, j2, rb);
         xi = 0.35f * exp2f(-(float)j2);
         invsig = 1.0f / (0.6f * xi); kc = xi * (float)NN;
         Hh = fminf(6.10f * (0.6f * xi) * (float)NN, 7967.0f);
@@ -625,17 +667,16 @@
                 int idx;
                 if (ring) idx = (kk - lo) & (Wd - 1);
                 else { idx = kk - lo; ok = (idx >= 0 && idx < Wd); }
-                v = ok ? __half22float2(Cw[cbase + idx]) : make_float2(0.f, 0.f);
+                v = ok ? h2f(Cw[cbase + idx]) : make_float2(0.f, 0.f);
             }
             float a = ((float)kk * (1.0f / (float)NN) - xi) * invsig;
             float wg = __expf(-0.5f * a * a) * 0.015625f;
             vr = v.x * wg; vi = v.y * wg;
         }
         int p = rev64(n2);
-        sre[(p << 6) + c] = vr;
-        sim[(p << 6) + c] = vi;
-    }
-    lds_dit<64, 6, 64, 1, false>(sre, sim, twt, t, 256);
+        sld[(p << 6) + c] = f2h(vr, vi);
+    }
+    lds_dit_pk<64, 6, 64, 1, false>(sld, twt, t, 256);
     {
         const int c = t & 63, r0 = t >> 6;
         float sA, cA, sD, cD;
@@ -645,8 +686,8 @@
         for (int it = 0; it < 16; ++it) {
             int row = (it << 2) + r0;
             int a = (row << 6) + c;
-            float rr = sre[a] * cA - sim[a] * sA;
-            sim[a] = sre[a] * sA + sim[a] * cA; sre[a] = rr;
+            float2 z = h2f(sld[a]);
+            sld[a] = f2h(z.x * cA - z.y * sA, z.x * sA + z.y * cA);
             float nc = cA * cD - sA * sD; sA = cA * sD + sA * cD; cA = nc;
         }
     }
@@ -655,24 +696,20 @@
     for (int it = 0; it < 16; ++it) {
         int flat = it * 256 + t;
         int c = flat & 63, row = flat >> 6;
-        Dh16[(size_t)r * 16384 + (row << 8) + (c0 + c)] =
-            __floats2half2_rn(sre[(row << 6) + c], sim[(row << 6) + c]);
-    }
-}
-
-__device__ void d_dec16_s2so(float* sm, int t, int blk, const __half2* __restrict__ Dh16,
+        Dh16[(size_t)r * 16384 + (row << 8) + (c0 + c)] = sld[(row << 6) + c];
+    }
+}
+
+__device__ void d_dec16_s2so(float* smf, int t, int blk, const __half2* __restrict__ Dh16,
                              float* __restrict__ S2acc)
 {
-    float* sre = sm; float* sim = sm + 4224;
-    float* wtab = sm + 8448;
+    __half2* sld = (__half2*)smf;
+    float* wtab = smf + 4320;
     const int r = blk >> 2;
     const int k2base = (blk & 3) << 4;
 #pragma unroll
-    for (int it = 0; it < 16; ++it) {
-        float2 v = __half22float2(Dh16[(size_t)r * 16384 + ((k2base + it) << 8) + t]);
-        sre[it * RSTR + SWZI(t, it)] = v.x;
-        sim[it * RSTR + SWZI(t, it)] = v.y;
-    }
+    for (int it = 0; it < 16; ++it)
+        sld[it * HRSTR + SWZI(t, it)] = Dh16[(size_t)r * 16384 + ((k2base + it) << 8) + t];
     if (t < 96) {
         int p = t / 6, dl = t % 6;
         float w = (float)(256 * (dl - 2) - 4 * (k2base + p));
@@ -680,13 +717,12 @@
     }
     __syncthreads();
     const int g = t >> 4, u = t & 15;
-    fft256_soa<1, false, 2, false, 3, 2>(sre + g * RSTR, sim + g * RSTR, u, 0, 0.f,
-                                         64.0f / (float)NN, g & 12, 15);
+    fft256_pk<1, false, 2, 3, 2>(sld + g * HRSTR, u, 0, 0.f, 64.0f / (float)NN, g & 12, 15);
     __syncthreads();
     float acc = 0.f;
 #pragma unroll
     for (int p = 0; p < 16; ++p) {
-        const float* row = sim + p * RSTR;
+        const float* row = (const float*)(sld + p * HRSTR);
 #pragma unroll
         for (int dl = 0; dl < 6; ++dl)
             acc = fmaf(row[t + 5 - dl], wtab[p * 6 + dl], acc);
@@ -694,35 +730,31 @@
     atomicAdd(&S2acc[(size_t)(192 + r) * 256 + t], acc * 4.0f);
 }
 
-__device__ void d_dec16_s2fo(float* sm, int t, int blk, const __half2* __restrict__ Dh16,
+__device__ void d_dec16_s2fo(float* smf, int t, int blk, const __half2* __restrict__ Dh16,
                              __half2* __restrict__ D2h16)
 {
-    float* sre = sm; float* sim = sm + 4224;
+    __half2* sld = (__half2*)smf;
     const int r = blk >> 2;
     const int k2base = (blk & 3) << 4;
 #pragma unroll
-    for (int it = 0; it < 16; ++it) {
-        float2 v = __half22float2(Dh16[(size_t)r * 16384 + ((k2base + it) << 8) + t]);
-        sre[it * RSTR + SWZI(t, it)] = v.x;
-        sim[it * RSTR + SWZI(t, it)] = v.y;
-    }
+    for (int it = 0; it < 16; ++it)
+        sld[it * HRSTR + SWZI(t, it)] = Dh16[(size_t)r * 16384 + ((k2base + it) << 8) + t];
     __syncthreads();
     const int g = t >> 4, u = t & 15;
-    float* rr = sre + g * RSTR; float* ri = sim + g * RSTR;
-    fft256_soa<1, false, 1, false, 0, 0>(rr, ri, u, 0, 0.f, 256.0f / (float)NN, g & 12, 15);
-    fft256_soa<-1, true, 0, true, 0, 0>(rr, ri, u, k2base + g, TWO_PI / 16384.0f, 1.f, g & 12, 15);
-    __syncthreads();
-#pragma unroll
-    for (int it = 0; it < 16; ++it) {
-        int a = it * RSTR + SWZI(t, it);
-        D2h16[(size_t)r * 16384 + ((k2base + it) << 8) + t] = __floats2half2_rn(sre[a], sim[a]);
-    }
-}
-
-__device__ void d_dec16_s3fo(float* sm, int t, int blk, const __half2* __restrict__ D2h16,
+    __half2* row = sld + g * HRSTR;
+    fft256_pk<1, false, 1, 0, 0>(row, u, 0, 0.f, 256.0f / (float)NN, g & 12, 15);
+    fft256_pk<-1, true, 0, 0, 0>(row, u, k2base + g, TWO_PI / 16384.0f, 1.f, g & 12, 15);
+    __syncthreads();
+#pragma unroll
+    for (int it = 0; it < 16; ++it)
+        D2h16[(size_t)r * 16384 + ((k2base + it) << 8) + t] = sld[it * HRSTR + SWZI(t, it)];
+}
+
+__device__ void d_dec16_s3fo(float* smf, int t, int blk, const __half2* __restrict__ D2h16,
                              __half2* __restrict__ Cw)
 {
-    float* sre = sm; float* sim = sm + 4096; float* twt = sm + 8192;
+    __half2* sld = (__half2*)smf;
+    float* twt = smf + 4224;
     const int r = blk >> 2;
     const int c0 = (blk & 3) << 6;
     const int j1 = 2 + (r >> 6), ql = r & 63;
@@ -731,11 +763,9 @@
     for (int it = 0; it < 16; ++it) {
         int flat = it * 256 + t;
         int c = flat & 63, m2 = flat >> 6;
-        float2 v = __half22float2(D2h16[(size_t)r * 16384 + (m2 << 8) + (c0 + c)]);
-        sre[(m2 << 6) + c] = v.x;
-        sim[(m2 << 6) + c] = v.y;
-    }
-    lds_dif<64, 6, 64, -1, false>(sre, sim, twt, t, 256);
+        sld[(m2 << 6) + c] = D2h16[(size_t)r * 16384 + (m2 << 8) + (c0 + c)];
+    }
+    lds_dif_pk<64, 6, 64, -1, false>(sld, twt, t, 256);
     const int lo = CLO[j1];
     const size_t rbase = COFF[j1] + (size_t)ql * 16384;
 #pragma unroll
@@ -745,17 +775,16 @@
         int kap = (c0 + c) + (rev64(p) << 8);
         int ks = (kap < 8192) ? kap : kap - 16384;
         int idx = (ks - lo) & 16383;
-        int a = (p << 6) + c;
-        Cw[rbase + idx] = __floats2half2_rn(sre[a], sim[a]);
-    }
-}
-
-__device__ void d_m4k_fo(float* sm, int t, int blk, const float2* __restrict__ XF,
+        Cw[rbase + idx] = sld[(p << 6) + c];
+    }
+}
+
+__device__ void d_m4k_fo(float* smf, int t, int blk, const float2* __restrict__ XF,
                          __half2* __restrict__ Cw)
 {
-    float* sre = sm; float* sim = sm + 4224; float* twt = sm + 8448;
-    const int q = blk;
-    const int j1 = 5 + (q >> 6), ql = q & 63;
+    __half2* sld = (__half2*)smf;
+    float* twt = smf + 4224;
+    const int j1 = 5 + (blk >> 6), ql = blk & 63;
     const int srow = ql >> 3;
     const int lam = j1 * 8 + (ql & 7);
     const float xi = 0.35f * exp2f(-(float)lam * 0.125f);
@@ -776,27 +805,26 @@
             vr = v.x * wg; vi = v.y * wg;
         }
         int p = rev16(it);
-        sre[p * RSTR + SWZI(t, p)] = vr;
-        sim[p * RSTR + SWZI(t, p)] = vi;
-    }
-    lds_dit<16, 8, RSTR, 1, true>(sre, sim, twt, t, 256);
+        sld[p * HRSTR + SWZI(t, p)] = f2h(vr, vi);
+    }
+    lds_dit_pk<16, 8, HRSTR, 1, true>(sld, twt, t, 256);
     {
         float sD, cD; __sincosf((TWO_PI / 4096.0f) * (float)t, &sD, &cD);
         float cA = 1.f, sA = 0.f;
 #pragma unroll
         for (int it = 0; it < 16; ++it) {
-            int a = it * RSTR + SWZI(t, it);
-            float rr = sre[a] * cA - sim[a] * sA;
-            sim[a] = sre[a] * sA + sim[a] * cA; sre[a] = rr;
+            int a = it * HRSTR + SWZI(t, it);
+            float2 z = h2f(sld[a]);
+            sld[a] = f2h(z.x * cA - z.y * sA, z.x * sA + z.y * cA);
             float nc = cA * cD - sA * sD; sA = cA * sD + sA * cD; cA = nc;
         }
     }
     __syncthreads();
     const int g = t >> 4, u = t & 15;
-    float* rr = sre + g * RSTR; float* ri = sim + g * RSTR;
-    fft256_soa<1, false, 1, false, 0, 0>(rr, ri, u, 0, 0.f, 16.0f / (float)NN, g & 12, 15);
-    fft256_soa<-1, true, 0, true, 0, 0>(rr, ri, u, g, TWO_PI / 4096.0f, 1.f, g & 12, 15);
-    lds_dif<16, 8, RSTR, -1, true>(sre, sim, twt, t, 256);
+    __half2* row = sld + g * HRSTR;
+    fft256_pk<1, false, 1, 0, 0>(row, u, 0, 0.f, 16.0f / (float)NN, g & 12, 15);
+    fft256_pk<-1, true, 0, 0, 0>(row, u, g, TWO_PI / 4096.0f, 1.f, g & 12, 15);
+    lds_dif_pk<16, 8, HRSTR, -1, true>(sld, twt, t, 256);
     const int lo = CLO[j1];
     const size_t rbase = COFF[j1] + (size_t)ql * 4096;
 #pragma unroll
@@ -804,18 +832,17 @@
         int kap = t + (rev16(it) << 8);
         int ks = (kap < 2048) ? kap : kap - 4096;
         int idx = (ks - lo) & 4095;
-        int a = it * RSTR + SWZI(t, it);
-        Cw[rbase + idx] = __floats2half2_rn(sre[a], sim[a]);
-    }
-}
-
-__device__ void d_m4k_so(float* sm, int t, int blk, const __half2* __restrict__ Cw,
+        Cw[rbase + idx] = sld[it * HRSTR + SWZI(t, it)];
+    }
+}
+
+__device__ void d_m4k_so(float* smf, int t, int blk, const __half2* __restrict__ Cw,
                          float* __restrict__ out)
 {
-    float* sre = sm; float* sim = sm + 4224;
-    float* twt = sm + 8448; float* wtab = sm + 8544;
-    const int q = blk;
-    const int pp = q >> 6, rb = q & 63;
+    __half2* sld = (__half2*)smf;
+    float* twt = smf + 4224;
+    float* wtab = smf + 4320;
+    const int pp = blk >> 6, rb = blk & 63;
     int j1, j2;
     if (pp < 5)       { j2 = 5; j1 = pp; }
     else if (pp < 11) { j2 = 6; j1 = pp - 5; }
@@ -838,42 +865,40 @@
             if (ring) idx = (kk - lo) & (Wd - 1);
             else { idx = kk - lo; ok = (idx >= 0 && idx < Wd); }
             if (ok) {
-                float2 v = __half22float2(Cw[cbase + idx]);
+                float2 v = h2f(Cw[cbase + idx]);
                 float a = ((float)kk * (1.0f / (float)NN) - xi2) * invsig;
                 float wg = __expf(-0.5f * a * a);
                 vr = v.x * wg; vi = v.y * wg;
             }
         }
         int p = rev16(it);
-        sre[p * RSTR + SWZI(t, p)] = vr;
-        sim[p * RSTR + SWZI(t, p)] = vi;
+        sld[p * HRSTR + SWZI(t, p)] = f2h(vr, vi);
     }
     if (t < 96) {
         int p = t / 6, dl = t % 6;
         float w = (float)(256 * (dl - 2) - 16 * p);
         wtab[p * 6 + dl] = 0.003426963f * __expf(-3.690276e-5f * w * w);
     }
-    lds_dit<16, 8, RSTR, 1, true>(sre, sim, twt, t, 256);
+    lds_dit_pk<16, 8, HRSTR, 1, true>(sld, twt, t, 256);
     {
         float sD, cD; __sincosf((TWO_PI / 4096.0f) * (float)t, &sD, &cD);
         float cA = 1.f, sA = 0.f;
 #pragma unroll
         for (int it = 0; it < 16; ++it) {
-            int a = it * RSTR + SWZI(t, it);
-            float rr = sre[a] * cA - sim[a] * sA;
-            sim[a] = sre[a] * sA + sim[a] * cA; sre[a] = rr;
+            int a = it * HRSTR + SWZI(t, it);
+            float2 z = h2f(sld[a]);
+            sld[a] = f2h(z.x * cA - z.y * sA, z.x * sA + z.y * cA);
             float nc = cA * cD - sA * sD; sA = cA * sD + sA * cD; cA = nc;
         }
     }
     __syncthreads();
     const int g = t >> 4, u = t & 15;
-    fft256_soa<1, false, 2, false, 3, 2>(sre + g * RSTR, sim + g * RSTR, u, 0, 0.f,
-                                         1.0f / (float)NN, g & 12, 15);
+    fft256_pk<1, false, 2, 3, 2>(sld + g * HRSTR, u, 0, 0.f, 1.0f / (float)NN, g & 12, 15);
     __syncthreads();
     float acc = 0.f;
 #pragma unroll
     for (int p = 0; p < 16; ++p) {
-        const float* row = sim + p * RSTR;
+        const float* row = (const float*)(sld + p * HRSTR);
 #pragma unroll
         for (int dl = 0; dl < 6; ++dl)
             acc = fmaf(row[t + 5 - dl], wtab[p * 6 + dl], acc);
@@ -889,34 +914,34 @@
 void fo_s1_kernel(const float2* __restrict__ XF, __half2* __restrict__ Cw,
                   __half2* __restrict__ DhB, __half2* __restrict__ Dh16)
 {
-    __shared__ float sm[8704];
+    __shared__ float smf[SM_FLOATS];
     const int t = threadIdx.x;
     const int b = blockIdx.x;
-    if (b < 192) d_m4k_fo(sm, t, b, XF, Cw);
-    else if (b < 960) d_dec16_s1<1>(sm, t, b - 192, XF, nullptr, Dh16);
-    else d_fo_stage1(sm, t, b - 960, XF, DhB);
+    if (b < 192) d_m4k_fo(smf, t, b, XF, Cw);
+    else if (b < 960) d_dec16_s1<1>(smf, t, b - 192, XF, nullptr, Dh16);
+    else d_fo_stage1(smf, t, b - 960, XF, DhB);
 }
 
 __global__ __launch_bounds__(256)
 void fo_s2_kernel(const __half2* __restrict__ DhB, const __half2* __restrict__ Dh16,
                   __half2* __restrict__ D2h, __half2* __restrict__ D2h16)
 {
-    __shared__ float sm[8704];
+    __shared__ float smf[SM_FLOATS];
     const int t = threadIdx.x;
     const int b = blockIdx.x;
-    if (b < 768) d_dec16_s2fo(sm, t, b, Dh16, D2h16);
-    else d_fo_mid(sm, t, b - 768, DhB, D2h);
+    if (b < 768) d_dec16_s2fo(smf, t, b, Dh16, D2h16);
+    else d_fo_mid(smf, t, b - 768, DhB, D2h);
 }
 
 __global__ __launch_bounds__(256)
 void fo_s3_kernel(const __half2* __restrict__ D2h, const __half2* __restrict__ D2h16,
                   __half2* __restrict__ Cw)
 {
-    __shared__ float sm[8704];
+    __shared__ float smf[SM_FLOATS];
     const int t = threadIdx.x;
     const int b = blockIdx.x;
-    if (b < 768) d_dec16_s3fo(sm, t, b, D2h16, Cw);
-    else d_fo_stage2(sm, t, b - 768, D2h, Cw);
+    if (b < 768) d_dec16_s3fo(smf, t, b, D2h16, Cw);
+    else d_fo_stage2(smf, t, b - 768, D2h, Cw);
 }
 
 __global__ __launch_bounds__(256)
@@ -924,24 +949,24 @@
                  __half2* __restrict__ DhS, __half2* __restrict__ Dh16so,
                  float* __restrict__ out)
 {
-    __shared__ float sm[8704];
+    __shared__ float smf[SM_FLOATS];
     const int t = threadIdx.x;
     const int b = blockIdx.x;
-    if (b < 1152) d_m4k_so(sm, t, b, Cw, out);
-    else if (b < 2944) d_dec16_s1<2>(sm, t, b - 1152, nullptr, Cw, Dh16so);
-    else if (b < 6016) d_so_stage1(sm, t, b - 2944, Cw, DhS);
-    else d_sfold(sm, t, b - 6016, XF, Cw, out);
+    if (b < 1152) d_m4k_so(smf, t, b, Cw, out);
+    else if (b < 2944) d_dec16_s1<2>(smf, t, b - 1152, nullptr, Cw, Dh16so);
+    else if (b < 6016) d_so_stage1(smf, t, b - 2944, Cw, DhS);
+    else d_sfold(smf, t, b - 6016, XF, Cw, out);
 }
 
 __global__ __launch_bounds__(256)
 void so_2_kernel(const __half2* __restrict__ DhS, const __half2* __restrict__ Dh16so,
                  float* __restrict__ S2acc)
 {
-    __shared__ float sm[8704];
+    __shared__ float smf[SM_FLOATS];
     const int t = threadIdx.x;
     const int b = blockIdx.x;
-    if (b < 1792) d_dec16_s2so(sm, t, b, Dh16so, S2acc);
-    else d_so_stage2(sm, t, b - 1792, DhS, S2acc);
+    if (b < 1792) d_dec16_s2so(smf, t, b, Dh16so, S2acc);
+    else d_so_stage2(smf, t, b - 1792, DhS, S2acc);
 }
 
 __global__ __launch_bounds__(256)
@@ -958,13 +983,6 @@
     out[((size_t)b * 289 + chan) * 256 + n] = logf(mag + 1e-8f);
 }
 
-__global__ void zero2_kernel(float* a, int na, float* b, int nb)
-{
-    int i = blockIdx.x * 256 + threadIdx.x;
-    if (i < na) a[i] = 0.f;
-    else if (i < na + nb) b[i - na] = 0.f;
-}
-
 extern "C" void kernel_launch(void* const* d_in, const int* in_sizes, int n_in,
                               void* d_out, int out_size, void* d_ws, size_t ws_size,
                               hipStream_t stream)
@@ -988,13 +1006,11 @@
     __half2* Dh16so = (__half2*)(sc + 50331648ul);
     float2*  Df     = (float2*)sc;
 
-    {
-        int nz = 8 * 289 * 256;
-        int na = 640 * 256;
-        zero2_kernel<<<(nz + na + 255) / 256, 256, 0, stream>>>(out + nz, nz, S2acc, na);
-    }
-
-    xf_stage1<<<8 * 16, 256, 0, stream>>>(x, Df);
+    const int nz = 8 * 289 * 256;
+    const int na = 640 * 256;
+    const int zb = (nz + na + 255) / 256;
+
+    xfz_kernel<<<128 + zb, 256, 0, stream>>>(x, Df, out + nz, nz, S2acc, na);
     xf_stage2<<<8 * 16, 256, 0, stream>>>(Df, XF);
 
     fo_s1_kernel<<<3008, 256, 0, stream>>>(XF, Cw, DhB, Dh16);
```

After: 363.3 us. 1.41x slower.
